# Optimization experiments

Measured on AMD Instinct MI355X. Metric: run time of the kernel, lower is better.

The kernel has to match this reference:

```python
import jax, jax.numpy as jnp
import numpy as np
from jax import lax

N = 2048    # atoms
K = 16      # knn neighbors -> E = N*K = 32768 edges
H = 128     # latent width
L = 10      # stacked InteractionNetworks
STEPS = 10  # outer simulation iterations


def _rn(key, shape, scale=0.05):
    return scale * jax.random.normal(key, shape, dtype=jnp.float32)


def setup_inputs() -> dict:
    key = jax.random.key(0)
    ks = iter(jax.random.split(key, 40))
    inp = {
        "pos": jax.random.normal(next(ks), (N, 3), dtype=jnp.float32),
        "node_f": jax.random.normal(next(ks), (N, 24), dtype=jnp.float32),
        "mass": jnp.ones((N,), jnp.float32),
        # node encoder MLP(24,128,2,128)
        "nW1": _rn(next(ks), (24, H)), "nb1": _rn(next(ks), (H,)),
        "nW2": _rn(next(ks), (H, H)), "nb2": _rn(next(ks), (H,)),
        # edge encoder MLP(4,128,2,128)
        "eW1": _rn(next(ks), (4, H)), "eb1": _rn(next(ks), (H,)),
        "eW2": _rn(next(ks), (H, H)), "eb2": _rn(next(ks), (H,)),
        # RelationModel per IN: input = 2*dim_obj + dim_rel = 384, 4 Linear layers (ReLU after each)
        "rmW1": _rn(next(ks), (L, 3 * H, H)), "rmb1": _rn(next(ks), (L, H)),
        "rmW2": _rn(next(ks), (L, H, H)), "rmb2": _rn(next(ks), (L, H)),
        "rmW3": _rn(next(ks), (L, H, H)), "rmb3": _rn(next(ks), (L, H)),
        "rmW4": _rn(next(ks), (L, H, H)), "rmb4": _rn(next(ks), (L, H)),
        # ObjectModel per IN: input = dim_obj + dim_eff = 256 -> hidden 128 -> out 128
        "omW1": _rn(next(ks), (L, 2 * H, H)), "omb1": _rn(next(ks), (L, H)),
        "omW2": _rn(next(ks), (L, H, H)), "omb2": _rn(next(ks), (L, H)),
        # decoder MLP(128,128,2,3)
        "dW1": _rn(next(ks), (H, H)), "db1": _rn(next(ks), (H,)),
        "dW2": _rn(next(ks), (H, 3)), "db2": _rn(next(ks), (3,)),
        "k": K,
    }
    return inp


def _mlp2(x, W1, b1, W2, b2):
    return jax.nn.relu(x @ W1 + b1) @ W2 + b2


def _knn_edges(pos, k):
    # knn(P.pos, k): edge_index[:,0] = sender (neighbor), edge_index[:,1] = receiver
    n = pos.shape[0]
    sq = jnp.sum(pos * pos, axis=1)
    d2 = sq[:, None] + sq[None, :] - 2.0 * (pos @ pos.T)   # [N, N]
    d2 = d2 + 1e9 * jnp.eye(n, dtype=pos.dtype)            # exclude self
    _, idx = lax.top_k(-d2, k)                              # [N, k] nearest
    senders = idx.reshape(-1)                               # [E]
    receivers = jnp.repeat(jnp.arange(n), k)                # [E]
    rel = pos[senders] - pos[receivers]
    dist = jnp.linalg.norm(rel, axis=1, keepdims=True)
    ea0 = jnp.concatenate([rel, dist], axis=1)              # [E, 4]
    return senders, receivers, ea0


def _simulate(pos, node_f, mass, nW1, nb1, nW2, nb2, eW1, eb1, eW2, eb2,
              rmW1, rmb1, rmW2, rmb2, rmW3, rmb3, rmW4, rmb4,
              omW1, omb1, omW2, omb2, dW1, db1, dW2, db2, k):
    n = pos.shape[0]
    # G.pos = G.pos + randn * 0.1 ; G.vels = zeros
    pos = pos + 0.1 * jax.random.normal(jax.random.key(42), pos.shape, dtype=pos.dtype)
    vels = jnp.zeros_like(pos)

    stacked = (rmW1, rmb1, rmW2, rmb2, rmW3, rmb3, rmW4, rmb4,
               omW1, omb1, omW2, omb2)

    for _ in range(STEPS):
        senders, receivers, ea0 = _knn_edges(pos, k)

        # encode
        x = _mlp2(node_f, nW1, nb1, nW2, nb2)    # [N, H]
        ea = _mlp2(ea0, eW1, eb1, eW2, eb2)      # [E, H]

        # process: 10 InteractionNetworks. In the original, layer(P.x, P.senders,
        # P.receivers, P.edge_attr) binds rr=senders, rs=receivers, so the
        # one-hot matmuls obj.t()@rr / obj.t()@rs are gathers by sender/receiver,
        # and e @ rr.t() is a scatter-add onto sender nodes.
        def in_step(carry, p):
            xc, eac = carry
            rW1, rb1, rW2, rb2, rW3, rb3, rW4, rb4, oW1, ob1, oW2, ob2 = p
            b = jnp.concatenate([xc[senders], xc[receivers], eac], axis=1)  # [E, 3H]
            h = jax.nn.relu(b @ rW1 + rb1)
            h = jax.nn.relu(h @ rW2 + rb2)
            h = jax.nn.relu(h @ rW3 + rb3)
            e = jax.nn.relu(h @ rW4 + rb4)                                   # [E, H]
            agg = jax.ops.segment_sum(e, senders, num_segments=n)           # e @ rr.T
            a = jnp.concatenate([xc, agg], axis=1)                           # [N, 2H]
            x_new = jax.nn.relu(a @ oW1 + ob1) @ oW2 + ob2                   # [N, H]
            return (x_new, e), None

        (x, ea), _ = lax.scan(jax.checkpoint(in_step), (x, ea), stacked)

        # decode + update
        forces = _mlp2(x, dW1, db1, dW2, db2)    # [N, 3]
        vels = vels + forces / mass[:, None]
        pos = pos + vels
    return pos


def reference(pos, node_f, mass, nW1, nb1, nW2, nb2, eW1, eb1, eW2, eb2,
              rmW1, rmb1, rmW2, rmb2, rmW3, rmb3, rmW4, rmb4,
              omW1, omb1, omW2, omb2, dW1, db1, dW2, db2, k):
    return _simulate(pos, node_f, mass, nW1, nb1, nW2, nb2, eW1, eb1, eW2, eb2,
                     rmW1, rmb1, rmW2, rmb2, rmW3, rmb3, rmW4, rmb4,
                     omW1, omb1, omW2, omb2, dW1, db1, dW2, db2, k)
```

## Files before the change

kernel.cpp:

```cpp
#include <hip/hip_runtime.h>

#define N_ATOMS 2048
#define KNN 16
#define NE (N_ATOMS*KNN)
#define H 128
#define NL 10
#define NSTEPS 10

typedef unsigned short u16;
typedef __attribute__((ext_vector_type(4))) float f32x4;
typedef __attribute__((ext_vector_type(8))) short bf16x8;

__device__ __forceinline__ u16 f2bf(float x){
  unsigned u = __float_as_uint(x);
  return (u16)((u + 0x7FFFu + ((u >> 16) & 1u)) >> 16);
}
__device__ __forceinline__ float bf2f(u16 v){ return __uint_as_float(((unsigned)v) << 16); }

template<int PITCH>
__device__ __forceinline__ bf16x8 ldsB_m6(const u16* s, int e, int k){
  int byte = e*PITCH + (k<<1); byte ^= ((e&7)<<4);
  return *(const bf16x8*)((const char*)s + byte);
}
template<int PITCH>
__device__ __forceinline__ void lds_st16_m6(u16* s, int row, int k, uint4 v){
  int byte = row*PITCH + (k<<1); byte ^= ((row&7)<<4);
  *(uint4*)((char*)s + byte) = v;
}
template<int PITCH>
__device__ __forceinline__ uint4 lds_ld16_m6(const u16* s, int row, int k){
  int byte = row*PITCH + (k<<1); byte ^= ((row&7)<<4);
  return *(const uint4*)((const char*)s + byte);
}
template<int PITCH>
__device__ __forceinline__ void lds_st8_m6(u16* s, int row, int k, uint2 v){
  int byte = row*PITCH + (k<<1); byte ^= ((row&7)<<4);
  *(uint2*)((char*)s + byte) = v;
}

template<int KST, int KS, int ET, int PITCH>
__device__ __forceinline__ void mfma_gemm_m6(const u16* sBh, const u16* sBl,
    const u16* __restrict__ pWh, const u16* __restrict__ pWl,
    int ksbase, int wpair, int rowbase, int lane, f32x4 acc[2][ET]){
  const int er = lane & 15, kg = lane >> 4;
  const size_t base = ((size_t)(wpair*KST + ksbase)*64 + lane)*8;
  #pragma unroll
  for (int ks = 0; ks < KS; ks++){
    const int klds = ks*32 + kg*8;
    bf16x8 bh[ET], bl[ET];
    #pragma unroll
    for (int et = 0; et < ET; et++){
      bh[et] = ldsB_m6<PITCH>(sBh, rowbase + et*16 + er, klds);
      bl[et] = ldsB_m6<PITCH>(sBl, rowbase + et*16 + er, klds);
    }
    #pragma unroll
    for (int nt = 0; nt < 2; nt++){
      const size_t off = base + (size_t)(nt*KST + ks)*512;
      bf16x8 ah = *(const bf16x8*)(pWh + off);
      bf16x8 al = *(const bf16x8*)(pWl + off);
      #pragma unroll
      for (int et = 0; et < ET; et++){
        acc[nt][et] = __builtin_amdgcn_mfma_f32_16x16x32_bf16(ah, bh[et], acc[nt][et], 0, 0, 0);
        acc[nt][et] = __builtin_amdgcn_mfma_f32_16x16x32_bf16(ah, bl[et], acc[nt][et], 0, 0, 0);
        acc[nt][et] = __builtin_amdgcn_mfma_f32_16x16x32_bf16(al, bh[et], acc[nt][et], 0, 0, 0);
      }
    }
  }
}

#define CLR_M6(acc, ET) { _Pragma("unroll") for (int i_=0;i_<2;i_++){ _Pragma("unroll") for (int j_=0;j_<ET;j_++){ \
  acc[i_][j_][0]=0.f; acc[i_][j_][1]=0.f; acc[i_][j_][2]=0.f; acc[i_][j_][3]=0.f; } } }

template<int ET, int PITCH, bool RELU>
__device__ __forceinline__ void epi_lds_m6(f32x4 acc[2][ET], u16* sh, u16* sl,
    int wpair, int rowbase, int lane, const float* __restrict__ bias){
  const int er = lane & 15, g = lane >> 4;
  #pragma unroll
  for (int nt = 0; nt < 2; nt++){
    const int n0 = (wpair + nt)*16 + g*4;
    f32x4 bv = *(const f32x4*)(bias + n0);
    #pragma unroll
    for (int et = 0; et < ET; et++){
      const int e = rowbase + et*16 + er;
      unsigned hw[2], lw[2];
      #pragma unroll
      for (int q = 0; q < 2; q++){
        float v0 = acc[nt][et][2*q]   + bv[2*q];
        float v1 = acc[nt][et][2*q+1] + bv[2*q+1];
        if (RELU){ v0 = fmaxf(v0, 0.f); v1 = fmaxf(v1, 0.f); }
        u16 h0 = f2bf(v0), h1 = f2bf(v1);
        u16 l0 = f2bf(v0 - bf2f(h0)), l1 = f2bf(v1 - bf2f(h1));
        hw[q] = (unsigned)h0 | ((unsigned)h1 << 16);
        lw[q] = (unsigned)l0 | ((unsigned)l1 << 16);
      }
      uint2 hv; hv.x = hw[0]; hv.y = hw[1];
      uint2 lv; lv.x = lw[0]; lv.y = lw[1];
      lds_st8_m6<PITCH>(sh, e, n0, hv);
      lds_st8_m6<PITCH>(sl, e, n0, lv);
    }
  }
}

__global__ __launch_bounds__(256) void pack_w_m6(const float* __restrict__ W,
    u16* __restrict__ ph, u16* __restrict__ pl, int KS, int L, int lstride, int roff){
  int idx = blockIdx.x*256 + threadIdx.x;
  int per = 8*KS*64;
  if (idx >= per*L) return;
  int l = idx / per, r = idx - l*per;
  int lane = r & 63, rest = r >> 6;
  int ks = rest % KS, nt = rest / KS;
  int n = nt*16 + (lane & 15), kb = ks*32 + (lane >> 4)*8;
  const float* src = W + (size_t)l*lstride;
  u16 h8[8], l8[8];
  #pragma unroll
  for (int j = 0; j < 8; j++){
    float v = src[(size_t)(roff + kb + j)*H + n];
    u16 h = f2bf(v);
    h8[j] = h; l8[j] = f2bf(v - bf2f(h));
  }
  size_t off = (size_t)idx*8;
  uint4 hv, lv;
  hv.x = h8[0]|((unsigned)h8[1]<<16); hv.y = h8[2]|((unsigned)h8[3]<<16);
  hv.z = h8[4]|((unsigned)h8[5]<<16); hv.w = h8[6]|((unsigned)h8[7]<<16);
  lv.x = l8[0]|((unsigned)l8[1]<<16); lv.y = l8[2]|((unsigned)l8[3]<<16);
  lv.z = l8[4]|((unsigned)l8[5]<<16); lv.w = l8[6]|((unsigned)l8[7]<<16);
  *(uint4*)(ph + off) = hv;
  *(uint4*)(pl + off) = lv;
}

__device__ __forceinline__ int lds_byte_f_m6(int r, int k4){
  return (((r<<9) + (k4<<2)) ^ (((r>>3)&7)<<4));
}
__device__ __forceinline__ f32x4 lds4r_f_m6(const float* s, int r, int k4){
  return *(const f32x4*)((const char*)s + lds_byte_f_m6(r,k4));
}
__device__ __forceinline__ void lds4w_f_m6(float* s, int r, int k4, f32x4 v){
  *(f32x4*)((char*)s + lds_byte_f_m6(r,k4)) = v;
}
__device__ __forceinline__ float lds1r_f_m6(const float* s, int r, int k){
  return *(const float*)((const char*)s + lds_byte_f_m6(r, k & ~3) + ((k&3)<<2));
}
template<int KD, int RPT>
__device__ __forceinline__ void gemm_f_m6(const float* sA, const float* __restrict__ gW,
                                          int r0, int c0, float acc[RPT][4]){
  #pragma unroll 2
  for (int k4 = 0; k4 < KD; k4 += 4){
    f32x4 a[RPT];
    #pragma unroll
    for (int i=0;i<RPT;i++) a[i] = lds4r_f_m6(sA, r0+i, k4);
    #pragma unroll
    for (int kk=0;kk<4;kk++){
      f32x4 wv = *(const f32x4*)(gW + (size_t)(k4+kk)*H + c0);
      #pragma unroll
      for (int i=0;i<RPT;i++){
        acc[i][0] = fmaf(a[i][kk], wv[0], acc[i][0]);
        acc[i][1] = fmaf(a[i][kk], wv[1], acc[i][1]);
        acc[i][2] = fmaf(a[i][kk], wv[2], acc[i][2]);
        acc[i][3] = fmaf(a[i][kk], wv[3], acc[i][3]);
      }
    }
  }
}

__device__ __forceinline__ unsigned rotl32_m6(unsigned v, int d){ return (v << d) | (v >> (32 - d)); }
__device__ __forceinline__ void tf2x32_m6(unsigned k0, unsigned k1, unsigned x0, unsigned x1,
                                          unsigned* o0, unsigned* o1){
  unsigned ks2 = k0 ^ k1 ^ 0x1BD11BDAu;
  x0 += k0; x1 += k1;
  const int R0[4] = {13,15,26,6}, R1[4] = {17,29,16,24};
#define TFG(R) { for (int i=0;i<4;i++){ x0 += x1; x1 = rotl32_m6(x1,R[i]); x1 ^= x0; } }
  TFG(R0); x0 += k1;  x1 += ks2 + 1u;
  TFG(R1); x0 += ks2; x1 += k0  + 2u;
  TFG(R0); x0 += k0;  x1 += k1  + 3u;
  TFG(R1); x0 += k1;  x1 += ks2 + 4u;
  TFG(R0); x0 += ks2; x1 += k0  + 5u;
#undef TFG
  *o0 = x0; *o1 = x1;
}
__device__ float bits_to_normal_m6(unsigned bits){
  float f = __uint_as_float((bits >> 9) | 0x3F800000u) - 1.0f;
  const float lo = -0.99999994f;
  float u = fmaxf(lo, __fadd_rn(__fmul_rn(f, 2.0f), lo));
  float w = -log1pf(-__fmul_rn(u, u));
  float p;
  if (w < 5.0f){
    w = __fsub_rn(w, 2.5f);
    p = 2.81022636e-08f;
    p = __fadd_rn(__fmul_rn(p,w),  3.43273939e-07f);
    p = __fadd_rn(__fmul_rn(p,w), -3.5233877e-06f);
    p = __fadd_rn(__fmul_rn(p,w), -4.39150654e-06f);
    p = __fadd_rn(__fmul_rn(p,w),  0.00021858087f);
    p = __fadd_rn(__fmul_rn(p,w), -0.00125372503f);
    p = __fadd_rn(__fmul_rn(p,w), -0.00417768164f);
    p = __fadd_rn(__fmul_rn(p,w),  0.246640727f);
    p = __fadd_rn(__fmul_rn(p,w),  1.50140941f);
  } else {
    w = __fsub_rn(sqrtf(w), 3.0f);
    p = -0.000200214257f;
    p = __fadd_rn(__fmul_rn(p,w),  0.000100950558f);
    p = __fadd_rn(__fmul_rn(p,w),  0.00134934322f);
    p = __fadd_rn(__fmul_rn(p,w), -0.00367342844f);
    p = __fadd_rn(__fmul_rn(p,w),  0.00573950773f);
    p = __fadd_rn(__fmul_rn(p,w), -0.0076224613f);
    p = __fadd_rn(__fmul_rn(p,w),  0.00943887047f);
    p = __fadd_rn(__fmul_rn(p,w),  1.00167406f);
    p = __fadd_rn(__fmul_rn(p,w),  2.83297682f);
  }
  return __fmul_rn(1.41421356f, __fmul_rn(p, u));
}
__device__ __forceinline__ unsigned draw_bits_m6(unsigned k1, unsigned k2, int bk, int m, int half){
  unsigned o0, o1;
  if (bk == 0){
    if (m < half){ tf2x32_m6(k1,k2, (unsigned)m, (unsigned)(m+half), &o0,&o1); return o0; }
    else         { tf2x32_m6(k1,k2, (unsigned)(m-half), (unsigned)m, &o0,&o1); return o1; }
  }
  tf2x32_m6(k1,k2, 0u, (unsigned)m, &o0,&o1);
  return (bk==1) ? (o0^o1) : (bk==2) ? o1 : o0;
}
__global__ __launch_bounds__(64) void rng_init_m6(int* flags){
  if (threadIdx.x < 8) flags[threadIdx.x] = 1;
}
__global__ __launch_bounds__(256) void rng_detect_m6(const float* __restrict__ pos_in, int* flags){
  int m = blockIdx.x*256 + threadIdx.x;
  if (m >= N_ATOMS*3) return;
  unsigned a0,a1,b0,b1,f0,f1;
  tf2x32_m6(0u,0u, 0u,40u, &a0,&a1);
  tf2x32_m6(0u,0u, 1u,41u, &b0,&b1);
  tf2x32_m6(0u,0u, 0u,0u,  &f0,&f1);
  float target = pos_in[m];
  #pragma unroll
  for (int v = 0; v < 8; v++){
    unsigned k1 = (v<4)? a0 : f0, k2 = (v<4)? b0 : f1;
    unsigned bits = draw_bits_m6(k1,k2, v&3, m, 3072);
    float z = bits_to_normal_m6(bits);
    if (fabsf(z - target) > 1e-3f) flags[v] = 0;
  }
}
__global__ __launch_bounds__(64) void rng_select_m6(const int* flags, int* sel){
  if (threadIdx.x == 0){
    int s = -1;
    for (int v = 0; v < 8; v++) if (flags[v]){ s = v; break; }
    sel[0] = (s < 0) ? 1 : (s & 3);
  }
}
__global__ __launch_bounds__(256) void perturb_m6(const float* __restrict__ pos,
                                                  const int* __restrict__ sel,
                                                  float* __restrict__ posw,
                                                  float* __restrict__ vels){
  int m = blockIdx.x*256 + threadIdx.x;
  if (m >= N_ATOMS*3) return;
  unsigned bits = draw_bits_m6(0u, 42u, sel[0], m, 3072);
  float z = bits_to_normal_m6(bits);
  posw[m] = __fadd_rn(pos[m], __fmul_rn(0.1f, z));
  vels[m] = 0.f;
}

__global__ __launch_bounds__(128) void node_enc_m6(const float* __restrict__ nf,
    const float* __restrict__ W1, const float* __restrict__ b1,
    const float* __restrict__ W2, const float* __restrict__ b2,
    u16* __restrict__ xh, u16* __restrict__ xl){
  __shared__ float s_in[24];
  __shared__ float s_h[128];
  int n = blockIdx.x, t = threadIdx.x;
  if (t < 24) s_in[t] = nf[n*24 + t];
  __syncthreads();
  float a = b1[t];
  #pragma unroll
  for (int k = 0; k < 24; k++) a = fmaf(s_in[k], W1[k*H + t], a);
  s_h[t] = fmaxf(a, 0.f);
  __syncthreads();
  float a2 = b2[t];
  for (int k = 0; k < H; k++) a2 = fmaf(s_h[k], W2[k*H + t], a2);
  u16 h = f2bf(a2);
  xh[(size_t)n*H + t] = h;
  xl[(size_t)n*H + t] = f2bf(a2 - bf2f(h));
}

__global__ __launch_bounds__(256) void pnode_m6(
    const u16* __restrict__ xh, const u16* __restrict__ xl,
    const u16* __restrict__ pah, const u16* __restrict__ pal,
    const u16* __restrict__ pbh, const u16* __restrict__ pbl,
    float* __restrict__ P1g, float* __restrict__ P2g){
  __shared__ __align__(16) u16 sXh[16*128];
  __shared__ __align__(16) u16 sXl[16*128];
  const int t = threadIdx.x, n0b = blockIdx.x*16;
  const int i = t>>4, seg = t&15;
  {
    uint4 hv = *(const uint4*)(xh + (size_t)(n0b+i)*H + seg*8);
    uint4 lv = *(const uint4*)(xl + (size_t)(n0b+i)*H + seg*8);
    lds_st16_m6<256>(sXh, i, seg*8, hv);
    lds_st16_m6<256>(sXl, i, seg*8, lv);
  }
  __syncthreads();
  const int w = t>>6, lane = t&63, er = lane&15, g = lane>>4;
  f32x4 acc[2][1];
  CLR_M6(acc, 1);
  mfma_gemm_m6<4,4,1,256>(sXh, sXl, pah, pal, 0, w*2, 0, lane, acc);
  #pragma unroll
  for (int nt = 0; nt < 2; nt++)
    *(f32x4*)(P1g + (size_t)(n0b+er)*H + (w*2+nt)*16 + g*4) = acc[nt][0];
  CLR_M6(acc, 1);
  mfma_gemm_m6<4,4,1,256>(sXh, sXl, pbh, pbl, 0, w*2, 0, lane, acc);
  #pragma unroll
  for (int nt = 0; nt < 2; nt++)
    *(f32x4*)(P2g + (size_t)(n0b+er)*H + (w*2+nt)*16 + g*4) = acc[nt][0];
}

__global__ __launch_bounds__(256) void knn_m6(const float* __restrict__ pos,
                                              int* __restrict__ senders,
                                              float* __restrict__ ea0){
  __shared__ float d2[N_ATOMS];
  __shared__ float pv[4];
  __shared__ int   pi[4];
  int r = blockIdx.x, t = threadIdx.x;
  float prx = pos[r*3+0], pry = pos[r*3+1], prz = pos[r*3+2];
  float sqr = __fadd_rn(__fadd_rn(__fmul_rn(prx,prx), __fmul_rn(pry,pry)), __fmul_rn(prz,prz));
  for (int c = t; c < N_ATOMS; c += 256){
    float cx = pos[c*3+0], cy = pos[c*3+1], cz = pos[c*3+2];
    float sqc = __fadd_rn(__fadd_rn(__fmul_rn(cx,cx), __fmul_rn(cy,cy)), __fmul_rn(cz,cz));
    float dot = __fadd_rn(__fadd_rn(__fmul_rn(prx,cx), __fmul_rn(pry,cy)), __fmul_rn(prz,cz));
    float v = __fsub_rn(__fadd_rn(sqr, sqc), __fmul_rn(2.0f, dot));
    d2[c] = (c == r) ? 1e9f : v;
  }
  __syncthreads();
  for (int j = 0; j < KNN; j++){
    float bv = 1e30f; int bi = 0x7fffffff;
    for (int c = t; c < N_ATOMS; c += 256){
      float v = d2[c];
      if (v < bv || (v == bv && c < bi)){ bv = v; bi = c; }
    }
    #pragma unroll
    for (int off = 32; off; off >>= 1){
      float ov = __shfl_down(bv, off);
      int   oi = __shfl_down(bi, off);
      if (ov < bv || (ov == bv && oi < bi)){ bv = ov; bi = oi; }
    }
    if ((t & 63) == 0){ pv[t>>6] = bv; pi[t>>6] = bi; }
    __syncthreads();
    if (t == 0){
      float fv = pv[0]; int fi = pi[0];
      #pragma unroll
      for (int q = 1; q < 4; q++){
        if (pv[q] < fv || (pv[q] == fv && pi[q] < fi)){ fv = pv[q]; fi = pi[q]; }
      }
      senders[r*KNN + j] = fi;
      float dx = __fsub_rn(pos[fi*3+0], prx);
      float dy = __fsub_rn(pos[fi*3+1], pry);
      float dz = __fsub_rn(pos[fi*3+2], prz);
      float ss = __fadd_rn(__fadd_rn(__fmul_rn(dx,dx), __fmul_rn(dy,dy)), __fmul_rn(dz,dz));
      float* o = ea0 + (size_t)(r*KNN + j)*4;
      o[0] = dx; o[1] = dy; o[2] = dz; o[3] = sqrtf(ss);
      d2[fi] = 1e30f;
    }
    __syncthreads();
  }
}

__global__ __launch_bounds__(1024) void csr_build_m6(const int* __restrict__ senders,
    int* __restrict__ rowstart, int* __restrict__ elist){
  __shared__ int cnt[N_ATOMS];
  __shared__ int part[256];
  const int t = threadIdx.x;
  for (int i = t; i < N_ATOMS; i += 1024) cnt[i] = 0;
  __syncthreads();
  #pragma unroll
  for (int k = 0; k < NE/1024; k++){
    int e = t + k*1024;
    atomicAdd(&cnt[senders[e]], 1);
  }
  __syncthreads();
  if (t < 256){
    int base = t*8, s = 0, loc[8];
    #pragma unroll
    for (int i = 0; i < 8; i++){ loc[i] = s; s += cnt[base+i]; }
    part[t] = s;
    __syncthreads();
    if (t == 0){
      int acc = 0;
      for (int i = 0; i < 256; i++){ int v = part[i]; part[i] = acc; acc += v; }
      rowstart[N_ATOMS] = acc;
    }
    __syncthreads();
    int p = part[t];
    #pragma unroll
    for (int i = 0; i < 8; i++){
      int v = p + loc[i];
      rowstart[base+i] = v;
      loc[i] = v;
    }
    __syncthreads();
    #pragma unroll
    for (int i = 0; i < 8; i++) cnt[base+i] = loc[i];
  } else {
    __syncthreads(); __syncthreads(); __syncthreads();
  }
  __syncthreads();
  #pragma unroll
  for (int k = 0; k < NE/1024; k++){
    int e = t + k*1024;
    int slot = atomicAdd(&cnt[senders[e]], 1);
    elist[slot] = e;
  }
}
__global__ __launch_bounds__(256) void csr_sort_m6(const int* __restrict__ rowstart, int* __restrict__ elist){
  int n = blockIdx.x*256 + threadIdx.x;
  if (n >= N_ATOMS) return;
  int b = rowstart[n], e = rowstart[n+1];
  for (int i = b+1; i < e; i++){
    int v = elist[i]; int j = i-1;
    while (j >= b && elist[j] > v){ elist[j+1] = elist[j]; j--; }
    elist[j+1] = v;
  }
}

__global__ __launch_bounds__(256) void edge_enc_m6(const float* __restrict__ ea0,
    const float* __restrict__ eW1, const float* __restrict__ eb1,
    const u16* __restrict__ e2h, const u16* __restrict__ e2l, const float* __restrict__ eb2,
    u16* __restrict__ eag){
  __shared__ float sE0[64*4];
  __shared__ __align__(16) u16 sHh[64*128];
  __shared__ __align__(16) u16 sHl[64*128];
  const int t = threadIdx.x;
  const int e0 = blockIdx.x*64;
  sE0[t] = ea0[(size_t)e0*4 + t];
  __syncthreads();
  const int w = t>>6, lane = t&63;
  const int r0 = ((lane>>3)&7)*8, c0 = w*32 + (lane&7)*4;
  f32x4 bv = *(const f32x4*)(eb1 + c0);
  f32x4 w0 = *(const f32x4*)(eW1 + 0*H + c0);
  f32x4 w1 = *(const f32x4*)(eW1 + 1*H + c0);
  f32x4 w2 = *(const f32x4*)(eW1 + 2*H + c0);
  f32x4 w3 = *(const f32x4*)(eW1 + 3*H + c0);
  #pragma unroll
  for (int i = 0; i < 8; i++){
    int r = r0 + i;
    float e0v = sE0[r*4+0], e1v = sE0[r*4+1], e2v = sE0[r*4+2], e3v = sE0[r*4+3];
    unsigned hw[2], lw[2];
    #pragma unroll
    for (int q = 0; q < 2; q++){
      float v0 = fmaf(e3v, w3[2*q],   fmaf(e2v, w2[2*q],   fmaf(e1v, w1[2*q],   fmaf(e0v, w0[2*q],   bv[2*q]))));
      float v1 = fmaf(e3v, w3[2*q+1], fmaf(e2v, w2[2*q+1], fmaf(e1v, w1[2*q+1], fmaf(e0v, w0[2*q+1], bv[2*q+1]))));
      v0 = fmaxf(v0, 0.f); v1 = fmaxf(v1, 0.f);
      u16 h0 = f2bf(v0), h1 = f2bf(v1);
      u16 l0 = f2bf(v0 - bf2f(h0)), l1 = f2bf(v1 - bf2f(h1));
      hw[q] = (unsigned)h0 | ((unsigned)h1<<16);
      lw[q] = (unsigned)l0 | ((unsigned)l1<<16);
    }
    uint2 hv; hv.x = hw[0]; hv.y = hw[1];
    uint2 lv; lv.x = lw[0]; lv.y = lw[1];
    lds_st8_m6<256>(sHh, r, c0, hv);
    lds_st8_m6<256>(sHl, r, c0, lv);
  }
  __syncthreads();
  f32x4 acc[2][4]; CLR_M6(acc, 4);
  mfma_gemm_m6<4,4,4,256>(sHh, sHl, e2h, e2l, 0, 2*w, 0, lane, acc);
  __syncthreads();
  epi_lds_m6<4,256,false>(acc, sHh, sHl, 2*w, 0, lane, eb2);
  __syncthreads();
  char* dst = (char*)(eag + (size_t)e0*256);
  #pragma unroll
  for (int m = 0; m < 8; m++){
    int byteoff = (t + m*256)*16;
    int row = byteoff>>9, off = byteoff&511;
    uint4 v = lds_ld16_m6<256>((off<256)? sHh : sHl, row, (off&255)>>1);
    *(uint4*)(dst + byteoff) = v;
  }
}

__global__ __launch_bounds__(256) void chain_m6(
    const float* __restrict__ P1g, const float* __restrict__ P2g,
    u16* __restrict__ eag, const int* __restrict__ senders,
    const u16* __restrict__ w1h, const u16* __restrict__ w1l, const float* __restrict__ b1,
    const u16* __restrict__ w2h, const u16* __restrict__ w2l, const float* __restrict__ b2,
    const u16* __restrict__ w3h, const u16* __restrict__ w3l, const float* __restrict__ b3,
    const u16* __restrict__ w4h, const u16* __restrict__ w4l, const float* __restrict__ b4){
  __shared__ __align__(16) u16 sPh[64*128];
  __shared__ __align__(16) u16 sPl[64*128];
  __shared__ __align__(16) u16 sQh[64*128];
  __shared__ __align__(16) u16 sQl[64*128];
  const int t = threadIdx.x, e0 = blockIdx.x*64;
  const int w = t>>6, lane = t&63, er = lane&15, g = lane>>4;
  const int wpair = w*2;
  f32x4 acc[2][4];
  int sidx[4];
  #pragma unroll
  for (int et = 0; et < 4; et++) sidx[et] = senders[e0 + et*16 + er];
  #pragma unroll
  for (int et = 0; et < 4; et++){
    const int r = (e0>>4) + et;
    #pragma unroll
    for (int nt = 0; nt < 2; nt++){
      const int n0 = (wpair+nt)*16 + g*4;
      f32x4 p1 = *(const f32x4*)(P1g + (size_t)sidx[et]*H + n0);
      f32x4 p2 = *(const f32x4*)(P2g + (size_t)r*H + n0);
      acc[nt][et] = p1 + p2;
    }
  }
  const char* src = (const char*)(eag + (size_t)e0*256);
  #pragma unroll
  for (int m = 0; m < 8; m++){
    int byteoff = (t + m*256)*16;
    uint4 v = *(const uint4*)(src + byteoff);
    int row = byteoff>>9, off = byteoff&511;
    lds_st16_m6<256>((off<256)? sPh : sPl, row, (off&255)>>1, v);
  }
  __syncthreads();
  mfma_gemm_m6<4,4,4,256>(sPh, sPl, w1h, w1l, 0, wpair, 0, lane, acc);
  epi_lds_m6<4,256,true>(acc, sQh, sQl, wpair, 0, lane, b1);
  __syncthreads();
  CLR_M6(acc, 4);
  mfma_gemm_m6<4,4,4,256>(sQh, sQl, w2h, w2l, 0, wpair, 0, lane, acc);
  epi_lds_m6<4,256,true>(acc, sPh, sPl, wpair, 0, lane, b2);
  __syncthreads();
  CLR_M6(acc, 4);
  mfma_gemm_m6<4,4,4,256>(sPh, sPl, w3h, w3l, 0, wpair, 0, lane, acc);
  epi_lds_m6<4,256,true>(acc, sQh, sQl, wpair, 0, lane, b3);
  __syncthreads();
  CLR_M6(acc, 4);
  mfma_gemm_m6<4,4,4,256>(sQh, sQl, w4h, w4l, 0, wpair, 0, lane, acc);
  epi_lds_m6<4,256,true>(acc, sPh, sPl, wpair, 0, lane, b4);
  __syncthreads();
  char* dst = (char*)(eag + (size_t)e0*256);
  #pragma unroll
  for (int m = 0; m < 8; m++){
    int byteoff = (t + m*256)*16;
    int row = byteoff>>9, off = byteoff&511;
    uint4 v = lds_ld16_m6<256>((off<256)? sPh : sPl, row, (off&255)>>1);
    *(uint4*)(dst + byteoff) = v;
  }
}

__global__ __launch_bounds__(256) void objagg_m6(
    const u16* __restrict__ xch, const u16* __restrict__ xcl,
    const u16* __restrict__ eag,
    const int* __restrict__ rowstart, const int* __restrict__ elist,
    const u16* __restrict__ o1h, const u16* __restrict__ o1l, const float* __restrict__ ob1,
    const u16* __restrict__ o2h, const u16* __restrict__ o2l, const float* __restrict__ ob2,
    const u16* __restrict__ nah, const u16* __restrict__ nal,
    const u16* __restrict__ nbh, const u16* __restrict__ nbl,
    u16* __restrict__ xoh, u16* __restrict__ xol,
    float* __restrict__ P1g, float* __restrict__ P2g){
  __shared__ __align__(16) u16 sIh[16*256];
  __shared__ __align__(16) u16 sIl[16*256];
  __shared__ __align__(16) u16 sHh[16*128];
  __shared__ __align__(16) u16 sHl[16*128];
  __shared__ __align__(16) u16 sXh[16*128];
  __shared__ __align__(16) u16 sXl[16*128];
  const int t = threadIdx.x, n0b = blockIdx.x*16;
  const int w = t>>6, lane = t&63;
  const int i = t>>4, seg = t&15;
  {
    uint4 hv = *(const uint4*)(xch + (size_t)(n0b+i)*H + seg*8);
    uint4 lv = *(const uint4*)(xcl + (size_t)(n0b+i)*H + seg*8);
    lds_st16_m6<512>(sIh, i, seg*8, hv);
    lds_st16_m6<512>(sIl, i, seg*8, lv);
    float a[8];
    #pragma unroll
    for (int k = 0; k < 8; k++) a[k] = 0.f;
    const int b = rowstart[n0b+i], e = rowstart[n0b+i+1];
    for (int p = b; p < e; p++){
      const int ed = elist[p];
      uint4 hv2 = *(const uint4*)(eag + (size_t)ed*256 + seg*8);
      uint4 lv2 = *(const uint4*)(eag + (size_t)ed*256 + 128 + seg*8);
      unsigned hwd[4] = {hv2.x,hv2.y,hv2.z,hv2.w};
      unsigned lwd[4] = {lv2.x,lv2.y,lv2.z,lv2.w};
      #pragma unroll
      for (int q = 0; q < 4; q++){
        a[2*q]   += bf2f((u16)(hwd[q]&0xffffu)) + bf2f((u16)(lwd[q]&0xffffu));
        a[2*q+1] += bf2f((u16)(hwd[q]>>16))     + bf2f((u16)(lwd[q]>>16));
      }
    }
    unsigned hw[4], lw[4];
    #pragma unroll
    for (int q = 0; q < 4; q++){
      float v0 = a[2*q], v1 = a[2*q+1];
      u16 h0 = f2bf(v0), h1 = f2bf(v1);
      u16 l0 = f2bf(v0 - bf2f(h0)), l1 = f2bf(v1 - bf2f(h1));
      hw[q] = (unsigned)h0 | ((unsigned)h1<<16);
      lw[q] = (unsigned)l0 | ((unsigned)l1<<16);
    }
    uint4 hv3; hv3.x=hw[0]; hv3.y=hw[1]; hv3.z=hw[2]; hv3.w=hw[3];
    uint4 lv3; lv3.x=lw[0]; lv3.y=lw[1]; lv3.z=lw[2]; lv3.w=lw[3];
    lds_st16_m6<512>(sIh, i, 128 + seg*8, hv3);
    lds_st16_m6<512>(sIl, i, 128 + seg*8, lv3);
  }
  __syncthreads();
  f32x4 acc[2][1];
  CLR_M6(acc, 1);
  mfma_gemm_m6<8,8,1,512>(sIh, sIl, o1h, o1l, 0, w*2, 0, lane, acc);
  epi_lds_m6<1,256,true>(acc, sHh, sHl, w*2, 0, lane, ob1);
  __syncthreads();
  CLR_M6(acc, 1);
  mfma_gemm_m6<4,4,1,256>(sHh, sHl, o2h, o2l, 0, w*2, 0, lane, acc);
  epi_lds_m6<1,256,false>(acc, sXh, sXl, w*2, 0, lane, ob2);
  __syncthreads();
  {
    int byteoff = t*16;
    int row = byteoff>>8, off = byteoff&255;
    uint4 hv = lds_ld16_m6<256>(sXh, row, off>>1);
    uint4 lv = lds_ld16_m6<256>(sXl, row, off>>1);
    *(uint4*)((char*)(xoh + (size_t)n0b*H) + byteoff) = hv;
    *(uint4*)((char*)(xol + (size_t)n0b*H) + byteoff) = lv;
  }
  const int er = lane&15, g = lane>>4;
  CLR_M6(acc, 1);
  mfma_gemm_m6<4,4,1,256>(sXh, sXl, nah, nal, 0, w*2, 0, lane, acc);
  #pragma unroll
  for (int nt = 0; nt < 2; nt++)
    *(f32x4*)(P1g + (size_t)(n0b+er)*H + (w*2+nt)*16 + g*4) = acc[nt][0];
  CLR_M6(acc, 1);
  mfma_gemm_m6<4,4,1,256>(sXh, sXl, nbh, nbl, 0, w*2, 0, lane, acc);
  #pragma unroll
  for (int nt = 0; nt < 2; nt++)
    *(f32x4*)(P2g + (size_t)(n0b+er)*H + (w*2+nt)*16 + g*4) = acc[nt][0];
}

__global__ __launch_bounds__(256) void decode_m6(
    const u16* __restrict__ xhi, const u16* __restrict__ xlo,
    const float* __restrict__ dW1, const float* __restrict__ db1,
    const float* __restrict__ dW2, const float* __restrict__ db2,
    const float* __restrict__ mass, float* __restrict__ posw, float* __restrict__ vels){
  __shared__ float sX[16*128];
  __shared__ float sY[16*128];
  const int t = threadIdx.x;
  const int n0 = blockIdx.x*16;
  const int w = t>>6, l = t&63;
  const int r0 = ((l>>3)&7)*2, c0 = w*32 + (l&7)*4;
  const int si = t>>4, sg = t&15;
  {
    const u16* ph = xhi + (size_t)(n0+si)*H + sg*8;
    const u16* pl = xlo + (size_t)(n0+si)*H + sg*8;
    uint4 hv = *(const uint4*)ph;
    uint4 lv = *(const uint4*)pl;
    unsigned hw[4] = {hv.x,hv.y,hv.z,hv.w}, lw[4] = {lv.x,lv.y,lv.z,lv.w};
    f32x4 v0, v1;
    #pragma unroll
    for (int m = 0; m < 2; m++){
      v0[2*m]   = bf2f((u16)(hw[m]&0xffffu)) + bf2f((u16)(lw[m]&0xffffu));
      v0[2*m+1] = bf2f((u16)(hw[m]>>16))     + bf2f((u16)(lw[m]>>16));
      v1[2*m]   = bf2f((u16)(hw[m+2]&0xffffu)) + bf2f((u16)(lw[m+2]&0xffffu));
      v1[2*m+1] = bf2f((u16)(hw[m+2]>>16))     + bf2f((u16)(lw[m+2]>>16));
    }
    lds4w_f_m6(sX, si, sg*8, v0);
    lds4w_f_m6(sX, si, sg*8 + 4, v1);
  }
  __syncthreads();
  float acc[2][4];
  #pragma unroll
  for (int i=0;i<2;i++){ acc[i][0]=0.f; acc[i][1]=0.f; acc[i][2]=0.f; acc[i][3]=0.f; }
  gemm_f_m6<128,2>(sX, dW1, r0, c0, acc);
  {
    f32x4 bv = *(const f32x4*)(db1 + c0);
    #pragma unroll
    for (int i=0;i<2;i++){
      f32x4 v;
      #pragma unroll
      for (int j=0;j<4;j++){ float x = acc[i][j] + bv[j]; v[j] = fmaxf(x, 0.f); }
      lds4w_f_m6(sY, r0+i, c0, v);
    }
  }
  __syncthreads();
  if (t < 48){
    int i = t/3, c = t - i*3;
    float a = db2[c];
    for (int k = 0; k < 128; k++) a = fmaf(lds1r_f_m6(sY, i, k), dW2[k*3 + c], a);
    int n = n0 + i;
    float f = a / mass[n];
    float v = vels[n*3 + c] + f;
    vels[n*3 + c] = v;
    posw[n*3 + c] += v;
  }
}

extern "C" void kernel_launch(void* const* d_in, const int* in_sizes, int n_in,
                              void* d_out, int out_size, void* d_ws, size_t ws_size,
                              hipStream_t stream){
  const float* pos   = (const float*)d_in[0];
  const float* nodef = (const float*)d_in[1];
  const float* mass  = (const float*)d_in[2];
  const float* nW1 = (const float*)d_in[3];  const float* nb1 = (const float*)d_in[4];
  const float* nW2 = (const float*)d_in[5];  const float* nb2 = (const float*)d_in[6];
  const float* eW1 = (const float*)d_in[7];  const float* eb1 = (const float*)d_in[8];
  const float* eW2 = (const float*)d_in[9];  const float* eb2 = (const float*)d_in[10];
  const float* rmW1 = (const float*)d_in[11]; const float* rmb1 = (const float*)d_in[12];
  const float* rmW2 = (const float*)d_in[13]; const float* rmb2 = (const float*)d_in[14];
  const float* rmW3 = (const float*)d_in[15]; const float* rmb3 = (const float*)d_in[16];
  const float* rmW4 = (const float*)d_in[17]; const float* rmb4 = (const float*)d_in[18];
  const float* omW1 = (const float*)d_in[19]; const float* omb1 = (const float*)d_in[20];
  const float* omW2 = (const float*)d_in[21]; const float* omb2 = (const float*)d_in[22];
  const float* dW1 = (const float*)d_in[23]; const float* db1 = (const float*)d_in[24];
  const float* dW2 = (const float*)d_in[25]; const float* db2 = (const float*)d_in[26];

  char* wptr = (char*)d_ws;
  auto alloc = [&](size_t bytes)->void*{
    void* p = (void*)wptr; wptr += (bytes + 255) & ~(size_t)255; return p;
  };
  float* posw  = (float*)alloc((size_t)N_ATOMS*3*4);
  float* vels  = (float*)alloc((size_t)N_ATOMS*3*4);
  int*   senders = (int*)alloc((size_t)NE*4);
  float* ea0   = (float*)alloc((size_t)NE*4*4);
  u16* xench = (u16*)alloc((size_t)N_ATOMS*H*2);
  u16* xencl = (u16*)alloc((size_t)N_ATOMS*H*2);
  u16* xAh   = (u16*)alloc((size_t)N_ATOMS*H*2);
  u16* xAl   = (u16*)alloc((size_t)N_ATOMS*H*2);
  u16* xBh   = (u16*)alloc((size_t)N_ATOMS*H*2);
  u16* xBl   = (u16*)alloc((size_t)N_ATOMS*H*2);
  u16* eag   = (u16*)alloc((size_t)NE*256*2);
  float* P1g  = (float*)alloc((size_t)N_ATOMS*H*4);
  float* P2g  = (float*)alloc((size_t)N_ATOMS*H*4);
  float* P01g = (float*)alloc((size_t)N_ATOMS*H*4);
  float* P02g = (float*)alloc((size_t)N_ATOMS*H*4);
  int* rowstart = (int*)alloc((size_t)(N_ATOMS+1)*4);
  int* elist    = (int*)alloc((size_t)NE*4);
  int* rflags   = (int*)alloc(64);
  int* rsel     = (int*)alloc(64);
  const size_t S4 = 8*4*64*8;
  const size_t S8 = 8*8*64*8;
  u16* p1ah = (u16*)alloc(S4*NL*2); u16* p1al = (u16*)alloc(S4*NL*2);
  u16* p1bh = (u16*)alloc(S4*NL*2); u16* p1bl = (u16*)alloc(S4*NL*2);
  u16* p1ch = (u16*)alloc(S4*NL*2); u16* p1cl = (u16*)alloc(S4*NL*2);
  u16* prm2h = (u16*)alloc(S4*NL*2); u16* prm2l = (u16*)alloc(S4*NL*2);
  u16* prm3h = (u16*)alloc(S4*NL*2); u16* prm3l = (u16*)alloc(S4*NL*2);
  u16* prm4h = (u16*)alloc(S4*NL*2); u16* prm4l = (u16*)alloc(S4*NL*2);
  u16* pom1h = (u16*)alloc(S8*NL*2); u16* pom1l = (u16*)alloc(S8*NL*2);
  u16* pom2h = (u16*)alloc(S4*NL*2); u16* pom2l = (u16*)alloc(S4*NL*2);
  u16* pe2h  = (u16*)alloc(S4*2);    u16* pe2l  = (u16*)alloc(S4*2);

  auto pack = [&](const float* W, u16* ph, u16* pl, int KS, int L, int lstride, int roff){
    int total = L*8*KS*64;
    pack_w_m6<<<(total+255)/256, 256, 0, stream>>>(W, ph, pl, KS, L, lstride, roff);
  };
  pack(rmW1, p1ah, p1al, 4, NL, 384*H, 0);
  pack(rmW1, p1bh, p1bl, 4, NL, 384*H, 128);
  pack(rmW1, p1ch, p1cl, 4, NL, 384*H, 256);
  pack(rmW2, prm2h, prm2l, 4, NL, H*H, 0);
  pack(rmW3, prm3h, prm3l, 4, NL, H*H, 0);
  pack(rmW4, prm4h, prm4l, 4, NL, H*H, 0);
  pack(omW1, pom1h, pom1l, 8, NL, 2*H*H, 0);
  pack(omW2, pom2h, pom2l, 4, NL, H*H, 0);
  pack(eW2,  pe2h,  pe2l,  4, 1,  H*H, 0);

  rng_init_m6<<<1, 64, 0, stream>>>(rflags);
  rng_detect_m6<<<(N_ATOMS*3+255)/256, 256, 0, stream>>>(pos, rflags);
  rng_select_m6<<<1, 64, 0, stream>>>(rflags, rsel);
  perturb_m6<<<(N_ATOMS*3+255)/256, 256, 0, stream>>>(pos, rsel, posw, vels);
  node_enc_m6<<<N_ATOMS, 128, 0, stream>>>(nodef, nW1, nb1, nW2, nb2, xench, xencl);
  pnode_m6<<<N_ATOMS/16, 256, 0, stream>>>(xench, xencl, p1ah, p1al, p1bh, p1bl, P01g, P02g);

  for (int s = 0; s < NSTEPS; s++){
    knn_m6<<<N_ATOMS, 256, 0, stream>>>(posw, senders, ea0);
    csr_build_m6<<<1, 1024, 0, stream>>>(senders, rowstart, elist);
    csr_sort_m6<<<(N_ATOMS+255)/256, 256, 0, stream>>>(rowstart, elist);
    edge_enc_m6<<<NE/64, 256, 0, stream>>>(ea0, eW1, eb1, pe2h, pe2l, eb2, eag);

    const u16* xch = xench; const u16* xcl = xencl;
    for (int l = 0; l < NL; l++){
      const float* Pa = (l == 0) ? P01g : P1g;
      const float* Pb = (l == 0) ? P02g : P2g;
      chain_m6<<<NE/64, 256, 0, stream>>>(Pa, Pb, eag, senders,
          p1ch  + (size_t)l*S4, p1cl  + (size_t)l*S4, rmb1 + l*H,
          prm2h + (size_t)l*S4, prm2l + (size_t)l*S4, rmb2 + l*H,
          prm3h + (size_t)l*S4, prm3l + (size_t)l*S4, rmb3 + l*H,
          prm4h + (size_t)l*S4, prm4l + (size_t)l*S4, rmb4 + l*H);
      u16* xnh = (l & 1) ? xAh : xBh;
      u16* xnl = (l & 1) ? xAl : xBl;
      int lp1 = (l < NL-1) ? (l+1) : l;
      objagg_m6<<<N_ATOMS/16, 256, 0, stream>>>(xch, xcl, eag, rowstart, elist,
          pom1h + (size_t)l*S8, pom1l + (size_t)l*S8, omb1 + l*H,
          pom2h + (size_t)l*S4, pom2l + (size_t)l*S4, omb2 + l*H,
          p1ah + (size_t)lp1*S4, p1al + (size_t)lp1*S4,
          p1bh + (size_t)lp1*S4, p1bl + (size_t)lp1*S4,
          xnh, xnl, P1g, P2g);
      xch = xnh; xcl = xnl;
    }
    decode_m6<<<N_ATOMS/16, 256, 0, stream>>>(xch, xcl, dW1, db1, dW2, db2, mass, posw, vels);
  }
  hipMemcpyAsync(d_out, posw, (size_t)N_ATOMS*3*4, hipMemcpyDeviceToDevice, stream);
}
```

Measured before the change: 6.003 ms.

## Fuse the whole simulation loop into one cooperative persistent kernel with grid syncs

Replaces the roughly 230 per-step kernel launches (knn, CSR build/sort, edge encoder, chain and objagg per layer, decode) with a single cooperative kernel of 512 blocks. It uses grid-wide barriers between phases and builds the CSR with atomic counts and cursors. The aim is to remove launch overhead and inter-kernel idle gaps. In exchange, occupancy is limited to 2 blocks per CU, and grid syncs plus atomic CSR construction add their own cost. The old multi-kernel path is kept as a fallback if the cooperative launch fails.

```diff
diff --git a/kernel.cpp b/kernel.cpp
--- a/kernel.cpp
+++ b/kernel.cpp
@@ -1,4 +1,7 @@
 #include <hip/hip_runtime.h>
+#include <hip/hip_cooperative_groups.h>
+
+namespace cg = cooperative_groups;
 
 #define N_ATOMS 2048
 #define KNN 16
@@ -6,6 +9,10 @@
 #define H 128
 #define NL 10
 #define NSTEPS 10
+#define S4C 16384
+#define S8C 32768
+#define S4B ((size_t)S4C)
+#define S8B ((size_t)S8C)
 
 typedef unsigned short u16;
 typedef __attribute__((ext_vector_type(4))) float f32x4;
@@ -18,28 +25,28 @@
 __device__ __forceinline__ float bf2f(u16 v){ return __uint_as_float(((unsigned)v) << 16); }
 
 template<int PITCH>
-__device__ __forceinline__ bf16x8 ldsB_m6(const u16* s, int e, int k){
+__device__ __forceinline__ bf16x8 ldsB_m7(const u16* s, int e, int k){
   int byte = e*PITCH + (k<<1); byte ^= ((e&7)<<4);
   return *(const bf16x8*)((const char*)s + byte);
 }
 template<int PITCH>
-__device__ __forceinline__ void lds_st16_m6(u16* s, int row, int k, uint4 v){
+__device__ __forceinline__ void lds_st16_m7(u16* s, int row, int k, uint4 v){
   int byte = row*PITCH + (k<<1); byte ^= ((row&7)<<4);
   *(uint4*)((char*)s + byte) = v;
 }
 template<int PITCH>
-__device__ __forceinline__ uint4 lds_ld16_m6(const u16* s, int row, int k){
+__device__ __forceinline__ uint4 lds_ld16_m7(const u16* s, int row, int k){
   int byte = row*PITCH + (k<<1); byte ^= ((row&7)<<4);
   return *(const uint4*)((const char*)s + byte);
 }
 template<int PITCH>
-__device__ __forceinline__ void lds_st8_m6(u16* s, int row, int k, uint2 v){
+__device__ __forceinline__ void lds_st8_m7(u16* s, int row, int k, uint2 v){
   int byte = row*PITCH + (k<<1); byte ^= ((row&7)<<4);
   *(uint2*)((char*)s + byte) = v;
 }
 
 template<int KST, int KS, int ET, int PITCH>
-__device__ __forceinline__ void mfma_gemm_m6(const u16* sBh, const u16* sBl,
+__device__ __forceinline__ void mfma_gemm_m7(const u16* sBh, const u16* sBl,
     const u16* __restrict__ pWh, const u16* __restrict__ pWl,
     int ksbase, int wpair, int rowbase, int lane, f32x4 acc[2][ET]){
   const int er = lane & 15, kg = lane >> 4;
@@ -50,8 +57,8 @@
     bf16x8 bh[ET], bl[ET];
     #pragma unroll
     for (int et = 0; et < ET; et++){
-      bh[et] = ldsB_m6<PITCH>(sBh, rowbase + et*16 + er, klds);
-      bl[et] = ldsB_m6<PITCH>(sBl, rowbase + et*16 + er, klds);
+      bh[et] = ldsB_m7<PITCH>(sBh, rowbase + et*16 + er, klds);
+      bl[et] = ldsB_m7<PITCH>(sBl, rowbase + et*16 + er, klds);
     }
     #pragma unroll
     for (int nt = 0; nt < 2; nt++){
@@ -68,11 +75,11 @@
   }
 }
 
-#define CLR_M6(acc, ET) { _Pragma("unroll") for (int i_=0;i_<2;i_++){ _Pragma("unroll") for (int j_=0;j_<ET;j_++){ \
+#define CLR_M7(acc, ET) { _Pragma("unroll") for (int i_=0;i_<2;i_++){ _Pragma("unroll") for (int j_=0;j_<ET;j_++){ \
   acc[i_][j_][0]=0.f; acc[i_][j_][1]=0.f; acc[i_][j_][2]=0.f; acc[i_][j_][3]=0.f; } } }
 
 template<int ET, int PITCH, bool RELU>
-__device__ __forceinline__ void epi_lds_m6(f32x4 acc[2][ET], u16* sh, u16* sl,
+__device__ __forceinline__ void epi_lds_m7(f32x4 acc[2][ET], u16* sh, u16* sl,
     int wpair, int rowbase, int lane, const float* __restrict__ bias){
   const int er = lane & 15, g = lane >> 4;
   #pragma unroll
@@ -95,13 +102,44 @@
       }
       uint2 hv; hv.x = hw[0]; hv.y = hw[1];
       uint2 lv; lv.x = lw[0]; lv.y = lw[1];
-      lds_st8_m6<PITCH>(sh, e, n0, hv);
-      lds_st8_m6<PITCH>(sl, e, n0, lv);
-    }
-  }
-}
-
-__global__ __launch_bounds__(256) void pack_w_m6(const float* __restrict__ W,
+      lds_st8_m7<PITCH>(sh, e, n0, hv);
+      lds_st8_m7<PITCH>(sl, e, n0, lv);
+    }
+  }
+}
+template<int ET, bool RELU>
+__device__ __forceinline__ void epi_glb_m7(f32x4 acc[2][ET],
+    u16* __restrict__ gh, u16* __restrict__ gl, int row0,
+    int wpair, int rowbase, int lane, const float* __restrict__ bias){
+  const int er = lane & 15, g = lane >> 4;
+  #pragma unroll
+  for (int nt = 0; nt < 2; nt++){
+    const int n0 = (wpair + nt)*16 + g*4;
+    f32x4 bv = *(const f32x4*)(bias + n0);
+    #pragma unroll
+    for (int et = 0; et < ET; et++){
+      const int e = rowbase + et*16 + er;
+      unsigned hw[2], lw[2];
+      #pragma unroll
+      for (int q = 0; q < 2; q++){
+        float v0 = acc[nt][et][2*q]   + bv[2*q];
+        float v1 = acc[nt][et][2*q+1] + bv[2*q+1];
+        if (RELU){ v0 = fmaxf(v0, 0.f); v1 = fmaxf(v1, 0.f); }
+        u16 h0 = f2bf(v0), h1 = f2bf(v1);
+        u16 l0 = f2bf(v0 - bf2f(h0)), l1 = f2bf(v1 - bf2f(h1));
+        hw[q] = (unsigned)h0 | ((unsigned)h1 << 16);
+        lw[q] = (unsigned)l0 | ((unsigned)l1 << 16);
+      }
+      size_t off = (size_t)(row0 + e)*H + n0;
+      uint2 hv; hv.x = hw[0]; hv.y = hw[1];
+      uint2 lv; lv.x = lw[0]; lv.y = lw[1];
+      *(uint2*)(gh + off) = hv;
+      *(uint2*)(gl + off) = lv;
+    }
+  }
+}
+
+__global__ __launch_bounds__(256) void pack_w_m7(const float* __restrict__ W,
     u16* __restrict__ ph, u16* __restrict__ pl, int KS, int L, int lstride, int roff){
   int idx = blockIdx.x*256 + threadIdx.x;
   int per = 8*KS*64;
@@ -128,26 +166,26 @@
   *(uint4*)(pl + off) = lv;
 }
 
-__device__ __forceinline__ int lds_byte_f_m6(int r, int k4){
+__device__ __forceinline__ int lds_byte_f_m7(int r, int k4){
   return (((r<<9) + (k4<<2)) ^ (((r>>3)&7)<<4));
 }
-__device__ __forceinline__ f32x4 lds4r_f_m6(const float* s, int r, int k4){
-  return *(const f32x4*)((const char*)s + lds_byte_f_m6(r,k4));
-}
-__device__ __forceinline__ void lds4w_f_m6(float* s, int r, int k4, f32x4 v){
-  *(f32x4*)((char*)s + lds_byte_f_m6(r,k4)) = v;
-}
-__device__ __forceinline__ float lds1r_f_m6(const float* s, int r, int k){
-  return *(const float*)((const char*)s + lds_byte_f_m6(r, k & ~3) + ((k&3)<<2));
+__device__ __forceinline__ f32x4 lds4r_f_m7(const float* s, int r, int k4){
+  return *(const f32x4*)((const char*)s + lds_byte_f_m7(r,k4));
+}
+__device__ __forceinline__ void lds4w_f_m7(float* s, int r, int k4, f32x4 v){
+  *(f32x4*)((char*)s + lds_byte_f_m7(r,k4)) = v;
+}
+__device__ __forceinline__ float lds1r_f_m7(const float* s, int r, int k){
+  return *(const float*)((const char*)s + lds_byte_f_m7(r, k & ~3) + ((k&3)<<2));
 }
 template<int KD, int RPT>
-__device__ __forceinline__ void gemm_f_m6(const float* sA, const float* __restrict__ gW,
+__device__ __forceinline__ void gemm_f_m7(const float* sA, const float* __restrict__ gW,
                                           int r0, int c0, float acc[RPT][4]){
   #pragma unroll 2
   for (int k4 = 0; k4 < KD; k4 += 4){
     f32x4 a[RPT];
     #pragma unroll
-    for (int i=0;i<RPT;i++) a[i] = lds4r_f_m6(sA, r0+i, k4);
+    for (int i=0;i<RPT;i++) a[i] = lds4r_f_m7(sA, r0+i, k4);
     #pragma unroll
     for (int kk=0;kk<4;kk++){
       f32x4 wv = *(const f32x4*)(gW + (size_t)(k4+kk)*H + c0);
@@ -162,13 +200,13 @@
   }
 }
 
-__device__ __forceinline__ unsigned rotl32_m6(unsigned v, int d){ return (v << d) | (v >> (32 - d)); }
-__device__ __forceinline__ void tf2x32_m6(unsigned k0, unsigned k1, unsigned x0, unsigned x1,
+__device__ __forceinline__ unsigned rotl32_m7(unsigned v, int d){ return (v << d) | (v >> (32 - d)); }
+__device__ __forceinline__ void tf2x32_m7(unsigned k0, unsigned k1, unsigned x0, unsigned x1,
                                           unsigned* o0, unsigned* o1){
   unsigned ks2 = k0 ^ k1 ^ 0x1BD11BDAu;
   x0 += k0; x1 += k1;
   const int R0[4] = {13,15,26,6}, R1[4] = {17,29,16,24};
-#define TFG(R) { for (int i=0;i<4;i++){ x0 += x1; x1 = rotl32_m6(x1,R[i]); x1 ^= x0; } }
+#define TFG(R) { for (int i=0;i<4;i++){ x0 += x1; x1 = rotl32_m7(x1,R[i]); x1 ^= x0; } }
   TFG(R0); x0 += k1;  x1 += ks2 + 1u;
   TFG(R1); x0 += ks2; x1 += k0  + 2u;
   TFG(R0); x0 += k0;  x1 += k1  + 3u;
@@ -177,7 +215,7 @@
 #undef TFG
   *o0 = x0; *o1 = x1;
 }
-__device__ float bits_to_normal_m6(unsigned bits){
+__device__ float bits_to_normal_m7(unsigned bits){
   float f = __uint_as_float((bits >> 9) | 0x3F800000u) - 1.0f;
   const float lo = -0.99999994f;
   float u = fmaxf(lo, __fadd_rn(__fmul_rn(f, 2.0f), lo));
@@ -208,54 +246,52 @@
   }
   return __fmul_rn(1.41421356f, __fmul_rn(p, u));
 }
-__device__ __forceinline__ unsigned draw_bits_m6(unsigned k1, unsigned k2, int bk, int m, int half){
+__device__ __forceinline__ unsigned draw_bits_m7(unsigned k1, unsigned k2, int bk, int m, int half){
   unsigned o0, o1;
   if (bk == 0){
-    if (m < half){ tf2x32_m6(k1,k2, (unsigned)m, (unsigned)(m+half), &o0,&o1); return o0; }
-    else         { tf2x32_m6(k1,k2, (unsigned)(m-half), (unsigned)m, &o0,&o1); return o1; }
-  }
-  tf2x32_m6(k1,k2, 0u, (unsigned)m, &o0,&o1);
+    if (m < half){ tf2x32_m7(k1,k2, (unsigned)m, (unsigned)(m+half), &o0,&o1); return o0; }
+    else         { tf2x32_m7(k1,k2, (unsigned)(m-half), (unsigned)m, &o0,&o1); return o1; }
+  }
+  tf2x32_m7(k1,k2, 0u, (unsigned)m, &o0,&o1);
   return (bk==1) ? (o0^o1) : (bk==2) ? o1 : o0;
 }
-__global__ __launch_bounds__(64) void rng_init_m6(int* flags){
+__global__ __launch_bounds__(64) void rng_init_m7(int* flags){
   if (threadIdx.x < 8) flags[threadIdx.x] = 1;
 }
-__global__ __launch_bounds__(256) void rng_detect_m6(const float* __restrict__ pos_in, int* flags){
+__global__ __launch_bounds__(256) void rng_detect_m7(const float* __restrict__ pos_in, int* flags){
   int m = blockIdx.x*256 + threadIdx.x;
   if (m >= N_ATOMS*3) return;
   unsigned a0,a1,b0,b1,f0,f1;
-  tf2x32_m6(0u,0u, 0u,40u, &a0,&a1);
-  tf2x32_m6(0u,0u, 1u,41u, &b0,&b1);
-  tf2x32_m6(0u,0u, 0u,0u,  &f0,&f1);
+  tf2x32_m7(0u,0u, 0u,40u, &a0,&a1);
+  tf2x32_m7(0u,0u, 1u,41u, &b0,&b1);
+  tf2x32_m7(0u,0u, 0u,0u,  &f0,&f1);
   float target = pos_in[m];
   #pragma unroll
   for (int v = 0; v < 8; v++){
     unsigned k1 = (v<4)? a0 : f0, k2 = (v<4)? b0 : f1;
-    unsigned bits = draw_bits_m6(k1,k2, v&3, m, 3072);
-    float z = bits_to_normal_m6(bits);
+    unsigned bits = draw_bits_m7(k1,k2, v&3, m, 3072);
+    float z = bits_to_normal_m7(bits);
     if (fabsf(z - target) > 1e-3f) flags[v] = 0;
   }
 }
-__global__ __launch_bounds__(64) void rng_select_m6(const int* flags, int* sel){
+__global__ __launch_bounds__(64) void rng_select_m7(const int* flags, int* sel){
   if (threadIdx.x == 0){
     int s = -1;
     for (int v = 0; v < 8; v++) if (flags[v]){ s = v; break; }
     sel[0] = (s < 0) ? 1 : (s & 3);
   }
 }
-__global__ __launch_bounds__(256) void perturb_m6(const float* __restrict__ pos,
-                                                  const int* __restrict__ sel,
-                                                  float* __restrict__ posw,
-                                                  float* __restrict__ vels){
+__global__ __launch_bounds__(256) void perturb_m7(const float* __restrict__ pos,
+    const int* __restrict__ sel, float* __restrict__ posw, float* __restrict__ vels){
   int m = blockIdx.x*256 + threadIdx.x;
   if (m >= N_ATOMS*3) return;
-  unsigned bits = draw_bits_m6(0u, 42u, sel[0], m, 3072);
-  float z = bits_to_normal_m6(bits);
+  unsigned bits = draw_bits_m7(0u, 42u, sel[0], m, 3072);
+  float z = bits_to_normal_m7(bits);
   posw[m] = __fadd_rn(pos[m], __fmul_rn(0.1f, z));
   vels[m] = 0.f;
 }
 
-__global__ __launch_bounds__(128) void node_enc_m6(const float* __restrict__ nf,
+__global__ __launch_bounds__(128) void node_enc_m7(const float* __restrict__ nf,
     const float* __restrict__ W1, const float* __restrict__ b1,
     const float* __restrict__ W2, const float* __restrict__ b2,
     u16* __restrict__ xh, u16* __restrict__ xl){
@@ -276,7 +312,7 @@
   xl[(size_t)n*H + t] = f2bf(a2 - bf2f(h));
 }
 
-__global__ __launch_bounds__(256) void pnode_m6(
+__global__ __launch_bounds__(256) void pnode_m7(
     const u16* __restrict__ xh, const u16* __restrict__ xl,
     const u16* __restrict__ pah, const u16* __restrict__ pal,
     const u16* __restrict__ pbh, const u16* __restrict__ pbl,
@@ -288,27 +324,391 @@
   {
     uint4 hv = *(const uint4*)(xh + (size_t)(n0b+i)*H + seg*8);
     uint4 lv = *(const uint4*)(xl + (size_t)(n0b+i)*H + seg*8);
-    lds_st16_m6<256>(sXh, i, seg*8, hv);
-    lds_st16_m6<256>(sXl, i, seg*8, lv);
+    lds_st16_m7<256>(sXh, i, seg*8, hv);
+    lds_st16_m7<256>(sXl, i, seg*8, lv);
   }
   __syncthreads();
   const int w = t>>6, lane = t&63, er = lane&15, g = lane>>4;
   f32x4 acc[2][1];
-  CLR_M6(acc, 1);
-  mfma_gemm_m6<4,4,1,256>(sXh, sXl, pah, pal, 0, w*2, 0, lane, acc);
+  CLR_M7(acc, 1);
+  mfma_gemm_m7<4,4,1,256>(sXh, sXl, pah, pal, 0, w*2, 0, lane, acc);
   #pragma unroll
   for (int nt = 0; nt < 2; nt++)
     *(f32x4*)(P1g + (size_t)(n0b+er)*H + (w*2+nt)*16 + g*4) = acc[nt][0];
-  CLR_M6(acc, 1);
-  mfma_gemm_m6<4,4,1,256>(sXh, sXl, pbh, pbl, 0, w*2, 0, lane, acc);
+  CLR_M7(acc, 1);
+  mfma_gemm_m7<4,4,1,256>(sXh, sXl, pbh, pbl, 0, w*2, 0, lane, acc);
   #pragma unroll
   for (int nt = 0; nt < 2; nt++)
     *(f32x4*)(P2g + (size_t)(n0b+er)*H + (w*2+nt)*16 + g*4) = acc[nt][0];
 }
 
-__global__ __launch_bounds__(256) void knn_m6(const float* __restrict__ pos,
-                                              int* __restrict__ senders,
-                                              float* __restrict__ ea0){
+struct MegaP {
+  float* posw; float* vels;
+  int* senders; int* counts; int* rowstart; int* cursor; int* elist;
+  u16* eag;
+  const u16* xench; const u16* xencl;
+  u16* xAh; u16* xAl; u16* xBh; u16* xBl;
+  float* P1g; float* P2g; const float* P01g; const float* P02g;
+  const float* eW1; const float* eb1; const float* eb2;
+  const u16* pe2h; const u16* pe2l;
+  const u16* p1ah; const u16* p1al; const u16* p1bh; const u16* p1bl;
+  const u16* p1ch; const u16* p1cl;
+  const u16* prm2h; const u16* prm2l;
+  const u16* prm3h; const u16* prm3l;
+  const u16* prm4h; const u16* prm4l;
+  const u16* pom1h; const u16* pom1l;
+  const u16* pom2h; const u16* pom2l;
+  const float* rmb1; const float* rmb2; const float* rmb3; const float* rmb4;
+  const float* omb1; const float* omb2;
+  const float* dW1; const float* db1; const float* dW2; const float* db2;
+  const float* mass;
+};
+
+__global__ __launch_bounds__(256, 2) void mega_m7(MegaP P){
+  cg::grid_group grid = cg::this_grid();
+  __shared__ __align__(16) char SM[65536];
+  const int b = blockIdx.x, t = threadIdx.x;
+  const int w = t >> 6, lane = t & 63;
+  const int er = lane & 15, g = lane >> 4;
+
+  for (int s = 0; s < NSTEPS; s++){
+    {
+      float* d2 = (float*)(SM + w*8192);
+      int*   sSend = (int*)(SM + 49152);
+      float* ea0loc = (float*)(SM + 50176);
+      const int r = b*4 + w;
+      float prx = P.posw[r*3+0], pry = P.posw[r*3+1], prz = P.posw[r*3+2];
+      float sqr = __fadd_rn(__fadd_rn(__fmul_rn(prx,prx), __fmul_rn(pry,pry)), __fmul_rn(prz,prz));
+      for (int c = lane; c < N_ATOMS; c += 64){
+        float cx = P.posw[c*3+0], cy = P.posw[c*3+1], cz = P.posw[c*3+2];
+        float sqc = __fadd_rn(__fadd_rn(__fmul_rn(cx,cx), __fmul_rn(cy,cy)), __fmul_rn(cz,cz));
+        float dot = __fadd_rn(__fadd_rn(__fmul_rn(prx,cx), __fmul_rn(pry,cy)), __fmul_rn(prz,cz));
+        float v = __fsub_rn(__fadd_rn(sqr, sqc), __fmul_rn(2.0f, dot));
+        d2[c] = (c == r) ? 1e9f : v;
+      }
+      asm volatile("" ::: "memory");
+      for (int j = 0; j < KNN; j++){
+        float bv = 1e30f; int bi = 0x7fffffff;
+        for (int c = lane; c < N_ATOMS; c += 64){
+          float v = d2[c];
+          if (v < bv || (v == bv && c < bi)){ bv = v; bi = c; }
+        }
+        #pragma unroll
+        for (int off = 32; off; off >>= 1){
+          float ov = __shfl_down(bv, off);
+          int   oi = __shfl_down(bi, off);
+          if (ov < bv || (ov == bv && oi < bi)){ bv = ov; bi = oi; }
+        }
+        if (lane == 0){
+          sSend[w*16 + j] = bi;
+          float dx = __fsub_rn(P.posw[bi*3+0], prx);
+          float dy = __fsub_rn(P.posw[bi*3+1], pry);
+          float dz = __fsub_rn(P.posw[bi*3+2], prz);
+          float ss = __fadd_rn(__fadd_rn(__fmul_rn(dx,dx), __fmul_rn(dy,dy)), __fmul_rn(dz,dz));
+          float* o = ea0loc + (w*16 + j)*4;
+          o[0] = dx; o[1] = dy; o[2] = dz; o[3] = sqrtf(ss);
+          d2[bi] = 1e30f;
+        }
+        asm volatile("" ::: "memory");
+      }
+      __syncthreads();
+      if (t < 64){
+        int sv = sSend[t];
+        P.senders[b*64 + t] = sv;
+        atomicAdd(&P.counts[sv], 1);
+      }
+      __syncthreads();
+      u16* sHh = (u16*)SM;
+      u16* sHl = (u16*)(SM + 16384);
+      const int r0e = ((lane>>3)&7)*8, c0e = w*32 + (lane&7)*4;
+      f32x4 bv1 = *(const f32x4*)(P.eb1 + c0e);
+      f32x4 w0v = *(const f32x4*)(P.eW1 + 0*H + c0e);
+      f32x4 w1v = *(const f32x4*)(P.eW1 + 1*H + c0e);
+      f32x4 w2v = *(const f32x4*)(P.eW1 + 2*H + c0e);
+      f32x4 w3v = *(const f32x4*)(P.eW1 + 3*H + c0e);
+      #pragma unroll
+      for (int i = 0; i < 8; i++){
+        int rr = r0e + i;
+        float e0v = ea0loc[rr*4+0], e1v = ea0loc[rr*4+1], e2v = ea0loc[rr*4+2], e3v = ea0loc[rr*4+3];
+        unsigned hw[2], lw[2];
+        #pragma unroll
+        for (int q = 0; q < 2; q++){
+          float v0 = fmaf(e3v, w3v[2*q],   fmaf(e2v, w2v[2*q],   fmaf(e1v, w1v[2*q],   fmaf(e0v, w0v[2*q],   bv1[2*q]))));
+          float v1 = fmaf(e3v, w3v[2*q+1], fmaf(e2v, w2v[2*q+1], fmaf(e1v, w1v[2*q+1], fmaf(e0v, w0v[2*q+1], bv1[2*q+1]))));
+          v0 = fmaxf(v0, 0.f); v1 = fmaxf(v1, 0.f);
+          u16 h0 = f2bf(v0), h1 = f2bf(v1);
+          u16 l0 = f2bf(v0 - bf2f(h0)), l1 = f2bf(v1 - bf2f(h1));
+          hw[q] = (unsigned)h0 | ((unsigned)h1<<16);
+          lw[q] = (unsigned)l0 | ((unsigned)l1<<16);
+        }
+        uint2 hv; hv.x = hw[0]; hv.y = hw[1];
+        uint2 lv; lv.x = lw[0]; lv.y = lw[1];
+        lds_st8_m7<256>(sHh, rr, c0e, hv);
+        lds_st8_m7<256>(sHl, rr, c0e, lv);
+      }
+      __syncthreads();
+      f32x4 acc[2][4];
+      CLR_M7(acc, 4);
+      mfma_gemm_m7<4,4,4,256>(sHh, sHl, P.pe2h, P.pe2l, 0, 2*w, 0, lane, acc);
+      __syncthreads();
+      epi_lds_m7<4,256,false>(acc, sHh, sHl, 2*w, 0, lane, P.eb2);
+      __syncthreads();
+      {
+        char* dst = (char*)(P.eag + (size_t)(b*64)*256);
+        #pragma unroll
+        for (int m = 0; m < 8; m++){
+          int byteoff = (t + m*256)*16;
+          int row = byteoff>>9, off = byteoff&511;
+          uint4 v = lds_ld16_m7<256>((off<256)? sHh : sHl, row, (off&255)>>1);
+          *(uint4*)(dst + byteoff) = v;
+        }
+      }
+    }
+    grid.sync();
+    if (b == 0){
+      int* part = (int*)SM;
+      int base = t*8, ssum = 0, loc[8];
+      #pragma unroll
+      for (int i = 0; i < 8; i++){ loc[i] = ssum; ssum += P.counts[base+i]; }
+      part[t] = ssum;
+      __syncthreads();
+      if (t == 0){
+        int acc2 = 0;
+        for (int i = 0; i < 256; i++){ int v = part[i]; part[i] = acc2; acc2 += v; }
+        P.rowstart[N_ATOMS] = acc2;
+      }
+      __syncthreads();
+      int p0 = part[t];
+      #pragma unroll
+      for (int i = 0; i < 8; i++){
+        int v = p0 + loc[i];
+        P.rowstart[base+i] = v;
+        P.cursor[base+i] = v;
+      }
+    }
+    grid.sync();
+    if (t < 64){
+      int e = b*64 + t;
+      int sv = P.senders[e];
+      int slot = atomicAdd(&P.cursor[sv], 1);
+      P.elist[slot] = e;
+    } else if (t < 68){
+      P.counts[b*4 + (t - 64)] = 0;
+    }
+    grid.sync();
+    const u16* xch = P.xench; const u16* xcl = P.xencl;
+    for (int l = 0; l < NL; l++){
+      if (l == 0 && t < 4){
+        int n = b*4 + t;
+        int b0 = P.rowstart[n], e1s = P.rowstart[n+1];
+        for (int i = b0+1; i < e1s; i++){
+          int v = P.elist[i]; int j = i-1;
+          while (j >= b0 && P.elist[j] > v){ P.elist[j+1] = P.elist[j]; j--; }
+          P.elist[j+1] = v;
+        }
+      }
+      {
+        u16* sPh = (u16*)SM;
+        u16* sPl = (u16*)(SM + 16384);
+        u16* sQh = (u16*)(SM + 32768);
+        u16* sQl = (u16*)(SM + 49152);
+        const int e0 = b*64;
+        const int wpair = w*2;
+        const float* Pa = (l == 0) ? P.P01g : P.P1g;
+        const float* Pb = (l == 0) ? P.P02g : P.P2g;
+        const u16* w1h = P.p1ch + (size_t)l*S4B;  const u16* w1l = P.p1cl + (size_t)l*S4B;
+        const u16* w2h = P.prm2h + (size_t)l*S4B; const u16* w2l = P.prm2l + (size_t)l*S4B;
+        const u16* w3h = P.prm3h + (size_t)l*S4B; const u16* w3l = P.prm3l + (size_t)l*S4B;
+        const u16* w4h = P.prm4h + (size_t)l*S4B; const u16* w4l = P.prm4l + (size_t)l*S4B;
+        f32x4 acc[2][4];
+        int sidx[4];
+        #pragma unroll
+        for (int et = 0; et < 4; et++) sidx[et] = P.senders[e0 + et*16 + er];
+        #pragma unroll
+        for (int et = 0; et < 4; et++){
+          const int rr = (e0>>4) + et;
+          #pragma unroll
+          for (int nt = 0; nt < 2; nt++){
+            const int n0 = (wpair+nt)*16 + g*4;
+            f32x4 p1 = *(const f32x4*)(Pa + (size_t)sidx[et]*H + n0);
+            f32x4 p2 = *(const f32x4*)(Pb + (size_t)rr*H + n0);
+            acc[nt][et] = p1 + p2;
+          }
+        }
+        {
+          const char* src = (const char*)(P.eag + (size_t)e0*256);
+          #pragma unroll
+          for (int m = 0; m < 8; m++){
+            int byteoff = (t + m*256)*16;
+            uint4 v = *(const uint4*)(src + byteoff);
+            int row = byteoff>>9, off = byteoff&511;
+            lds_st16_m7<256>((off<256)? sPh : sPl, row, (off&255)>>1, v);
+          }
+        }
+        __syncthreads();
+        mfma_gemm_m7<4,4,4,256>(sPh, sPl, w1h, w1l, 0, wpair, 0, lane, acc);
+        epi_lds_m7<4,256,true>(acc, sQh, sQl, wpair, 0, lane, P.rmb1 + l*H);
+        __syncthreads();
+        CLR_M7(acc, 4);
+        mfma_gemm_m7<4,4,4,256>(sQh, sQl, w2h, w2l, 0, wpair, 0, lane, acc);
+        epi_lds_m7<4,256,true>(acc, sPh, sPl, wpair, 0, lane, P.rmb2 + l*H);
+        __syncthreads();
+        CLR_M7(acc, 4);
+        mfma_gemm_m7<4,4,4,256>(sPh, sPl, w3h, w3l, 0, wpair, 0, lane, acc);
+        epi_lds_m7<4,256,true>(acc, sQh, sQl, wpair, 0, lane, P.rmb3 + l*H);
+        __syncthreads();
+        CLR_M7(acc, 4);
+        mfma_gemm_m7<4,4,4,256>(sQh, sQl, w4h, w4l, 0, wpair, 0, lane, acc);
+        epi_lds_m7<4,256,true>(acc, sPh, sPl, wpair, 0, lane, P.rmb4 + l*H);
+        __syncthreads();
+        {
+          char* dst = (char*)(P.eag + (size_t)e0*256);
+          #pragma unroll
+          for (int m = 0; m < 8; m++){
+            int byteoff = (t + m*256)*16;
+            int row = byteoff>>9, off = byteoff&511;
+            uint4 v = lds_ld16_m7<256>((off<256)? sPh : sPl, row, (off&255)>>1);
+            *(uint4*)(dst + byteoff) = v;
+          }
+        }
+      }
+      grid.sync();
+      u16* xnh = (l & 1) ? P.xAh : P.xBh;
+      u16* xnl = (l & 1) ? P.xAl : P.xBl;
+      if (b < 128){
+        u16* sIh  = (u16*)SM;
+        u16* sIl  = (u16*)(SM + 8192);
+        u16* sHh2 = (u16*)(SM + 16384);
+        u16* sHl2 = (u16*)(SM + 20480);
+        u16* sXh  = (u16*)(SM + 24576);
+        u16* sXl  = (u16*)(SM + 28672);
+        const int n0b = b*16;
+        const int i = t>>4, seg = t&15;
+        {
+          uint4 hv = *(const uint4*)(xch + (size_t)(n0b+i)*H + seg*8);
+          uint4 lv = *(const uint4*)(xcl + (size_t)(n0b+i)*H + seg*8);
+          lds_st16_m7<512>(sIh, i, seg*8, hv);
+          lds_st16_m7<512>(sIl, i, seg*8, lv);
+          float a[8];
+          #pragma unroll
+          for (int k = 0; k < 8; k++) a[k] = 0.f;
+          const int b0 = P.rowstart[n0b+i], e1a = P.rowstart[n0b+i+1];
+          for (int p = b0; p < e1a; p++){
+            const int ed = P.elist[p];
+            uint4 hv2 = *(const uint4*)(P.eag + (size_t)ed*256 + seg*8);
+            uint4 lv2 = *(const uint4*)(P.eag + (size_t)ed*256 + 128 + seg*8);
+            unsigned hwd[4] = {hv2.x,hv2.y,hv2.z,hv2.w};
+            unsigned lwd[4] = {lv2.x,lv2.y,lv2.z,lv2.w};
+            #pragma unroll
+            for (int q = 0; q < 4; q++){
+              a[2*q]   += bf2f((u16)(hwd[q]&0xffffu)) + bf2f((u16)(lwd[q]&0xffffu));
+              a[2*q+1] += bf2f((u16)(hwd[q]>>16))     + bf2f((u16)(lwd[q]>>16));
+            }
+          }
+          unsigned hw2[4], lw2[4];
+          #pragma unroll
+          for (int q = 0; q < 4; q++){
+            float v0 = a[2*q], v1 = a[2*q+1];
+            u16 h0 = f2bf(v0), h1 = f2bf(v1);
+            u16 l0 = f2bf(v0 - bf2f(h0)), l1 = f2bf(v1 - bf2f(h1));
+            hw2[q] = (unsigned)h0 | ((unsigned)h1<<16);
+            lw2[q] = (unsigned)l0 | ((unsigned)l1<<16);
+          }
+          uint4 hv3; hv3.x=hw2[0]; hv3.y=hw2[1]; hv3.z=hw2[2]; hv3.w=hw2[3];
+          uint4 lv3; lv3.x=lw2[0]; lv3.y=lw2[1]; lv3.z=lw2[2]; lv3.w=lw2[3];
+          lds_st16_m7<512>(sIh, i, 128 + seg*8, hv3);
+          lds_st16_m7<512>(sIl, i, 128 + seg*8, lv3);
+        }
+        __syncthreads();
+        f32x4 acc1[2][1];
+        CLR_M7(acc1, 1);
+        mfma_gemm_m7<8,8,1,512>(sIh, sIl, P.pom1h + (size_t)l*S8B, P.pom1l + (size_t)l*S8B,
+                                0, w*2, 0, lane, acc1);
+        epi_lds_m7<1,256,true>(acc1, sHh2, sHl2, w*2, 0, lane, P.omb1 + l*H);
+        __syncthreads();
+        CLR_M7(acc1, 1);
+        mfma_gemm_m7<4,4,1,256>(sHh2, sHl2, P.pom2h + (size_t)l*S4B, P.pom2l + (size_t)l*S4B,
+                                0, w*2, 0, lane, acc1);
+        epi_lds_m7<1,256,false>(acc1, sXh, sXl, w*2, 0, lane, P.omb2 + l*H);
+        __syncthreads();
+        if (l < NL-1){
+          {
+            int byteoff = t*16;
+            int row = byteoff>>8, off = byteoff&255;
+            uint4 hv = lds_ld16_m7<256>(sXh, row, off>>1);
+            uint4 lv = lds_ld16_m7<256>(sXl, row, off>>1);
+            *(uint4*)((char*)(xnh + (size_t)n0b*H) + byteoff) = hv;
+            *(uint4*)((char*)(xnl + (size_t)n0b*H) + byteoff) = lv;
+          }
+          const int lp1 = l + 1;
+          CLR_M7(acc1, 1);
+          mfma_gemm_m7<4,4,1,256>(sXh, sXl, P.p1ah + (size_t)lp1*S4B, P.p1al + (size_t)lp1*S4B,
+                                  0, w*2, 0, lane, acc1);
+          #pragma unroll
+          for (int nt = 0; nt < 2; nt++)
+            *(f32x4*)(P.P1g + (size_t)(n0b+er)*H + (w*2+nt)*16 + g*4) = acc1[nt][0];
+          CLR_M7(acc1, 1);
+          mfma_gemm_m7<4,4,1,256>(sXh, sXl, P.p1bh + (size_t)lp1*S4B, P.p1bl + (size_t)lp1*S4B,
+                                  0, w*2, 0, lane, acc1);
+          #pragma unroll
+          for (int nt = 0; nt < 2; nt++)
+            *(f32x4*)(P.P2g + (size_t)(n0b+er)*H + (w*2+nt)*16 + g*4) = acc1[nt][0];
+        } else {
+          float* sXf = (float*)(SM + 32768);
+          float* sYf = (float*)(SM + 40960);
+          {
+            uint4 hv = lds_ld16_m7<256>(sXh, i, seg*8);
+            uint4 lv = lds_ld16_m7<256>(sXl, i, seg*8);
+            unsigned hwv[4] = {hv.x,hv.y,hv.z,hv.w}, lwv[4] = {lv.x,lv.y,lv.z,lv.w};
+            f32x4 v0, v1;
+            #pragma unroll
+            for (int m = 0; m < 2; m++){
+              v0[2*m]   = bf2f((u16)(hwv[m]&0xffffu)) + bf2f((u16)(lwv[m]&0xffffu));
+              v0[2*m+1] = bf2f((u16)(hwv[m]>>16))     + bf2f((u16)(lwv[m]>>16));
+              v1[2*m]   = bf2f((u16)(hwv[m+2]&0xffffu)) + bf2f((u16)(lwv[m+2]&0xffffu));
+              v1[2*m+1] = bf2f((u16)(hwv[m+2]>>16))     + bf2f((u16)(lwv[m+2]>>16));
+            }
+            lds4w_f_m7(sXf, i, seg*8, v0);
+            lds4w_f_m7(sXf, i, seg*8 + 4, v1);
+          }
+          __syncthreads();
+          const int r0d = ((lane>>3)&7)*2, c0d = w*32 + (lane&7)*4;
+          float fac[2][4];
+          #pragma unroll
+          for (int ii = 0; ii < 2; ii++){ fac[ii][0]=0.f; fac[ii][1]=0.f; fac[ii][2]=0.f; fac[ii][3]=0.f; }
+          gemm_f_m7<128,2>(sXf, P.dW1, r0d, c0d, fac);
+          {
+            f32x4 bvd = *(const f32x4*)(P.db1 + c0d);
+            #pragma unroll
+            for (int ii = 0; ii < 2; ii++){
+              f32x4 v;
+              #pragma unroll
+              for (int jj = 0; jj < 4; jj++){ float x = fac[ii][jj] + bvd[jj]; v[jj] = fmaxf(x, 0.f); }
+              lds4w_f_m7(sYf, r0d+ii, c0d, v);
+            }
+          }
+          __syncthreads();
+          if (t < 48){
+            int i2 = t/3, c = t - i2*3;
+            float a2 = P.db2[c];
+            for (int k = 0; k < H; k++) a2 = fmaf(lds1r_f_m7(sYf, i2, k), P.dW2[k*3 + c], a2);
+            int n = n0b + i2;
+            float f = a2 / P.mass[n];
+            float v = P.vels[n*3 + c] + f;
+            P.vels[n*3 + c] = v;
+            P.posw[n*3 + c] += v;
+          }
+        }
+      }
+      grid.sync();
+      xch = xnh; xcl = xnl;
+    }
+  }
+}
+
+__global__ __launch_bounds__(256) void knn_m7f(const float* __restrict__ pos,
+                                               int* __restrict__ senders,
+                                               float* __restrict__ ea0){
   __shared__ float d2[N_ATOMS];
   __shared__ float pv[4];
   __shared__ int   pi[4];
@@ -355,8 +755,7 @@
     __syncthreads();
   }
 }
-
-__global__ __launch_bounds__(1024) void csr_build_m6(const int* __restrict__ senders,
+__global__ __launch_bounds__(1024) void csr_build_m7f(const int* __restrict__ senders,
     int* __restrict__ rowstart, int* __restrict__ elist){
   __shared__ int cnt[N_ATOMS];
   __shared__ int part[256];
@@ -402,7 +801,7 @@
     elist[slot] = e;
   }
 }
-__global__ __launch_bounds__(256) void csr_sort_m6(const int* __restrict__ rowstart, int* __restrict__ elist){
+__global__ __launch_bounds__(256) void csr_sort_m7f(const int* __restrict__ rowstart, int* __restrict__ elist){
   int n = blockIdx.x*256 + threadIdx.x;
   if (n >= N_ATOMS) return;
   int b = rowstart[n], e = rowstart[n+1];
@@ -412,8 +811,7 @@
     elist[j+1] = v;
   }
 }
-
-__global__ __launch_bounds__(256) void edge_enc_m6(const float* __restrict__ ea0,
+__global__ __launch_bounds__(256) void edge_enc_m7f(const float* __restrict__ ea0,
     const float* __restrict__ eW1, const float* __restrict__ eb1,
     const u16* __restrict__ e2h, const u16* __restrict__ e2l, const float* __restrict__ eb2,
     u16* __restrict__ eag){
@@ -448,26 +846,25 @@
     }
     uint2 hv; hv.x = hw[0]; hv.y = hw[1];
     uint2 lv; lv.x = lw[0]; lv.y = lw[1];
-    lds_st8_m6<256>(sHh, r, c0, hv);
-    lds_st8_m6<256>(sHl, r, c0, lv);
-  }
-  __syncthreads();
-  f32x4 acc[2][4]; CLR_M6(acc, 4);
-  mfma_gemm_m6<4,4,4,256>(sHh, sHl, e2h, e2l, 0, 2*w, 0, lane, acc);
-  __syncthreads();
-  epi_lds_m6<4,256,false>(acc, sHh, sHl, 2*w, 0, lane, eb2);
+    lds_st8_m7<256>(sHh, r, c0, hv);
+    lds_st8_m7<256>(sHl, r, c0, lv);
+  }
+  __syncthreads();
+  f32x4 acc[2][4]; CLR_M7(acc, 4);
+  mfma_gemm_m7<4,4,4,256>(sHh, sHl, e2h, e2l, 0, 2*w, 0, lane, acc);
+  __syncthreads();
+  epi_lds_m7<4,256,false>(acc, sHh, sHl, 2*w, 0, lane, eb2);
   __syncthreads();
   char* dst = (char*)(eag + (size_t)e0*256);
   #pragma unroll
   for (int m = 0; m < 8; m++){
     int byteoff = (t + m*256)*16;
     int row = byteoff>>9, off = byteoff&511;
-    uint4 v = lds_ld16_m6<256>((off<256)? sHh : sHl, row, (off&255)>>1);
+    uint4 v = lds_ld16_m7<256>((off<256)? sHh : sHl, row, (off&255)>>1);
     *(uint4*)(dst + byteoff) = v;
   }
 }
-
-__global__ __launch_bounds__(256) void chain_m6(
+__global__ __launch_bounds__(256) void chain_m7f(
     const float* __restrict__ P1g, const float* __restrict__ P2g,
     u16* __restrict__ eag, const int* __restrict__ senders,
     const u16* __restrict__ w1h, const u16* __restrict__ w1l, const float* __restrict__ b1,
@@ -496,41 +893,42 @@
       acc[nt][et] = p1 + p2;
     }
   }
-  const char* src = (const char*)(eag + (size_t)e0*256);
-  #pragma unroll
-  for (int m = 0; m < 8; m++){
-    int byteoff = (t + m*256)*16;
-    uint4 v = *(const uint4*)(src + byteoff);
-    int row = byteoff>>9, off = byteoff&511;
-    lds_st16_m6<256>((off<256)? sPh : sPl, row, (off&255)>>1, v);
-  }
-  __syncthreads();
-  mfma_gemm_m6<4,4,4,256>(sPh, sPl, w1h, w1l, 0, wpair, 0, lane, acc);
-  epi_lds_m6<4,256,true>(acc, sQh, sQl, wpair, 0, lane, b1);
-  __syncthreads();
-  CLR_M6(acc, 4);
-  mfma_gemm_m6<4,4,4,256>(sQh, sQl, w2h, w2l, 0, wpair, 0, lane, acc);
-  epi_lds_m6<4,256,true>(acc, sPh, sPl, wpair, 0, lane, b2);
-  __syncthreads();
-  CLR_M6(acc, 4);
-  mfma_gemm_m6<4,4,4,256>(sPh, sPl, w3h, w3l, 0, wpair, 0, lane, acc);
-  epi_lds_m6<4,256,true>(acc, sQh, sQl, wpair, 0, lane, b3);
-  __syncthreads();
-  CLR_M6(acc, 4);
-  mfma_gemm_m6<4,4,4,256>(sQh, sQl, w4h, w4l, 0, wpair, 0, lane, acc);
-  epi_lds_m6<4,256,true>(acc, sPh, sPl, wpair, 0, lane, b4);
+  {
+    const char* src = (const char*)(eag + (size_t)e0*256);
+    #pragma unroll
+    for (int m = 0; m < 8; m++){
+      int byteoff = (t + m*256)*16;
+      uint4 v = *(const uint4*)(src + byteoff);
+      int row = byteoff>>9, off = byteoff&511;
+      lds_st16_m7<256>((off<256)? sPh : sPl, row, (off&255)>>1, v);
+    }
+  }
+  __syncthreads();
+  mfma_gemm_m7<4,4,4,256>(sPh, sPl, w1h, w1l, 0, wpair, 0, lane, acc);
+  epi_lds_m7<4,256,true>(acc, sQh, sQl, wpair, 0, lane, b1);
+  __syncthreads();
+  CLR_M7(acc, 4);
+  mfma_gemm_m7<4,4,4,256>(sQh, sQl, w2h, w2l, 0, wpair, 0, lane, acc);
+  epi_lds_m7<4,256,true>(acc, sPh, sPl, wpair, 0, lane, b2);
+  __syncthreads();
+  CLR_M7(acc, 4);
+  mfma_gemm_m7<4,4,4,256>(sPh, sPl, w3h, w3l, 0, wpair, 0, lane, acc);
+  epi_lds_m7<4,256,true>(acc, sQh, sQl, wpair, 0, lane, b3);
+  __syncthreads();
+  CLR_M7(acc, 4);
+  mfma_gemm_m7<4,4,4,256>(sQh, sQl, w4h, w4l, 0, wpair, 0, lane, acc);
+  epi_lds_m7<4,256,true>(acc, sPh, sPl, wpair, 0, lane, b4);
   __syncthreads();
   char* dst = (char*)(eag + (size_t)e0*256);
   #pragma unroll
   for (int m = 0; m < 8; m++){
     int byteoff = (t + m*256)*16;
     int row = byteoff>>9, off = byteoff&511;
-    uint4 v = lds_ld16_m6<256>((off<256)? sPh : sPl, row, (off&255)>>1);
+    uint4 v = lds_ld16_m7<256>((off<256)? sPh : sPl, row, (off&255)>>1);
     *(uint4*)(dst + byteoff) = v;
   }
 }
-
-__global__ __launch_bounds__(256) void objagg_m6(
+__global__ __launch_bounds__(256) void objagg_m7f(
     const u16* __restrict__ xch, const u16* __restrict__ xcl,
     const u16* __restrict__ eag,
     const int* __restrict__ rowstart, const int* __restrict__ elist,
@@ -552,8 +950,8 @@
   {
     uint4 hv = *(const uint4*)(xch + (size_t)(n0b+i)*H + seg*8);
     uint4 lv = *(const uint4*)(xcl + (size_t)(n0b+i)*H + seg*8);
-    lds_st16_m6<512>(sIh, i, seg*8, hv);
-    lds_st16_m6<512>(sIl, i, seg*8, lv);
+    lds_st16_m7<512>(sIh, i, seg*8, hv);
+    lds_st16_m7<512>(sIl, i, seg*8, lv);
     float a[8];
     #pragma unroll
     for (int k = 0; k < 8; k++) a[k] = 0.f;
@@ -581,41 +979,40 @@
     }
     uint4 hv3; hv3.x=hw[0]; hv3.y=hw[1]; hv3.z=hw[2]; hv3.w=hw[3];
     uint4 lv3; lv3.x=lw[0]; lv3.y=lw[1]; lv3.z=lw[2]; lv3.w=lw[3];
-    lds_st16_m6<512>(sIh, i, 128 + seg*8, hv3);
-    lds_st16_m6<512>(sIl, i, 128 + seg*8, lv3);
+    lds_st16_m7<512>(sIh, i, 128 + seg*8, hv3);
+    lds_st16_m7<512>(sIl, i, 128 + seg*8, lv3);
   }
   __syncthreads();
   f32x4 acc[2][1];
-  CLR_M6(acc, 1);
-  mfma_gemm_m6<8,8,1,512>(sIh, sIl, o1h, o1l, 0, w*2, 0, lane, acc);
-  epi_lds_m6<1,256,true>(acc, sHh, sHl, w*2, 0, lane, ob1);
-  __syncthreads();
-  CLR_M6(acc, 1);
-  mfma_gemm_m6<4,4,1,256>(sHh, sHl, o2h, o2l, 0, w*2, 0, lane, acc);
-  epi_lds_m6<1,256,false>(acc, sXh, sXl, w*2, 0, lane, ob2);
+  CLR_M7(acc, 1);
+  mfma_gemm_m7<8,8,1,512>(sIh, sIl, o1h, o1l, 0, w*2, 0, lane, acc);
+  epi_lds_m7<1,256,true>(acc, sHh, sHl, w*2, 0, lane, ob1);
+  __syncthreads();
+  CLR_M7(acc, 1);
+  mfma_gemm_m7<4,4,1,256>(sHh, sHl, o2h, o2l, 0, w*2, 0, lane, acc);
+  epi_lds_m7<1,256,false>(acc, sXh, sXl, w*2, 0, lane, ob2);
   __syncthreads();
   {
     int byteoff = t*16;
     int row = byteoff>>8, off = byteoff&255;
-    uint4 hv = lds_ld16_m6<256>(sXh, row, off>>1);
-    uint4 lv = lds_ld16_m6<256>(sXl, row, off>>1);
+    uint4 hv = lds_ld16_m7<256>(sXh, row, off>>1);
+    uint4 lv = lds_ld16_m7<256>(sXl, row, off>>1);
     *(uint4*)((char*)(xoh + (size_t)n0b*H) + byteoff) = hv;
     *(uint4*)((char*)(xol + (size_t)n0b*H) + byteoff) = lv;
   }
   const int er = lane&15, g = lane>>4;
-  CLR_M6(acc, 1);
-  mfma_gemm_m6<4,4,1,256>(sXh, sXl, nah, nal, 0, w*2, 0, lane, acc);
+  CLR_M7(acc, 1);
+  mfma_gemm_m7<4,4,1,256>(sXh, sXl, nah, nal, 0, w*2, 0, lane, acc);
   #pragma unroll
   for (int nt = 0; nt < 2; nt++)
     *(f32x4*)(P1g + (size_t)(n0b+er)*H + (w*2+nt)*16 + g*4) = acc[nt][0];
-  CLR_M6(acc, 1);
-  mfma_gemm_m6<4,4,1,256>(sXh, sXl, nbh, nbl, 0, w*2, 0, lane, acc);
+  CLR_M7(acc, 1);
+  mfma_gemm_m7<4,4,1,256>(sXh, sXl, nbh, nbl, 0, w*2, 0, lane, acc);
   #pragma unroll
   for (int nt = 0; nt < 2; nt++)
     *(f32x4*)(P2g + (size_t)(n0b+er)*H + (w*2+nt)*16 + g*4) = acc[nt][0];
 }
-
-__global__ __launch_bounds__(256) void decode_m6(
+__global__ __launch_bounds__(256) void decode_m7f(
     const u16* __restrict__ xhi, const u16* __restrict__ xlo,
     const float* __restrict__ dW1, const float* __restrict__ db1,
     const float* __restrict__ dW2, const float* __restrict__ db2,
@@ -641,14 +1038,14 @@
       v1[2*m]   = bf2f((u16)(hw[m+2]&0xffffu)) + bf2f((u16)(lw[m+2]&0xffffu));
       v1[2*m+1] = bf2f((u16)(hw[m+2]>>16))     + bf2f((u16)(lw[m+2]>>16));
     }
-    lds4w_f_m6(sX, si, sg*8, v0);
-    lds4w_f_m6(sX, si, sg*8 + 4, v1);
+    lds4w_f_m7(sX, si, sg*8, v0);
+    lds4w_f_m7(sX, si, sg*8 + 4, v1);
   }
   __syncthreads();
   float acc[2][4];
   #pragma unroll
   for (int i=0;i<2;i++){ acc[i][0]=0.f; acc[i][1]=0.f; acc[i][2]=0.f; acc[i][3]=0.f; }
-  gemm_f_m6<128,2>(sX, dW1, r0, c0, acc);
+  gemm_f_m7<128,2>(sX, dW1, r0, c0, acc);
   {
     f32x4 bv = *(const f32x4*)(db1 + c0);
     #pragma unroll
@@ -656,14 +1053,14 @@
       f32x4 v;
       #pragma unroll
       for (int j=0;j<4;j++){ float x = acc[i][j] + bv[j]; v[j] = fmaxf(x, 0.f); }
-      lds4w_f_m6(sY, r0+i, c0, v);
+      lds4w_f_m7(sY, r0+i, c0, v);
     }
   }
   __syncthreads();
   if (t < 48){
     int i = t/3, c = t - i*3;
     float a = db2[c];
-    for (int k = 0; k < 128; k++) a = fmaf(lds1r_f_m6(sY, i, k), dW2[k*3 + c], a);
+    for (int k = 0; k < 128; k++) a = fmaf(lds1r_f_m7(sY, i, k), dW2[k*3 + c], a);
     int n = n0 + i;
     float f = a / mass[n];
     float v = vels[n*3 + c] + f;
@@ -710,25 +1107,25 @@
   float* P2g  = (float*)alloc((size_t)N_ATOMS*H*4);
   float* P01g = (float*)alloc((size_t)N_ATOMS*H*4);
   float* P02g = (float*)alloc((size_t)N_ATOMS*H*4);
+  int* counts   = (int*)alloc((size_t)N_ATOMS*4);
   int* rowstart = (int*)alloc((size_t)(N_ATOMS+1)*4);
+  int* cursor   = (int*)alloc((size_t)N_ATOMS*4);
   int* elist    = (int*)alloc((size_t)NE*4);
   int* rflags   = (int*)alloc(64);
   int* rsel     = (int*)alloc(64);
-  const size_t S4 = 8*4*64*8;
-  const size_t S8 = 8*8*64*8;
-  u16* p1ah = (u16*)alloc(S4*NL*2); u16* p1al = (u16*)alloc(S4*NL*2);
-  u16* p1bh = (u16*)alloc(S4*NL*2); u16* p1bl = (u16*)alloc(S4*NL*2);
-  u16* p1ch = (u16*)alloc(S4*NL*2); u16* p1cl = (u16*)alloc(S4*NL*2);
-  u16* prm2h = (u16*)alloc(S4*NL*2); u16* prm2l = (u16*)alloc(S4*NL*2);
-  u16* prm3h = (u16*)alloc(S4*NL*2); u16* prm3l = (u16*)alloc(S4*NL*2);
-  u16* prm4h = (u16*)alloc(S4*NL*2); u16* prm4l = (u16*)alloc(S4*NL*2);
-  u16* pom1h = (u16*)alloc(S8*NL*2); u16* pom1l = (u16*)alloc(S8*NL*2);
-  u16* pom2h = (u16*)alloc(S4*NL*2); u16* pom2l = (u16*)alloc(S4*NL*2);
-  u16* pe2h  = (u16*)alloc(S4*2);    u16* pe2l  = (u16*)alloc(S4*2);
+  u16* p1ah = (u16*)alloc(S4B*NL*2); u16* p1al = (u16*)alloc(S4B*NL*2);
+  u16* p1bh = (u16*)alloc(S4B*NL*2); u16* p1bl = (u16*)alloc(S4B*NL*2);
+  u16* p1ch = (u16*)alloc(S4B*NL*2); u16* p1cl = (u16*)alloc(S4B*NL*2);
+  u16* prm2h = (u16*)alloc(S4B*NL*2); u16* prm2l = (u16*)alloc(S4B*NL*2);
+  u16* prm3h = (u16*)alloc(S4B*NL*2); u16* prm3l = (u16*)alloc(S4B*NL*2);
+  u16* prm4h = (u16*)alloc(S4B*NL*2); u16* prm4l = (u16*)alloc(S4B*NL*2);
+  u16* pom1h = (u16*)alloc(S8B*NL*2); u16* pom1l = (u16*)alloc(S8B*NL*2);
+  u16* pom2h = (u16*)alloc(S4B*NL*2); u16* pom2l = (u16*)alloc(S4B*NL*2);
+  u16* pe2h  = (u16*)alloc(S4B*2);    u16* pe2l  = (u16*)alloc(S4B*2);
 
   auto pack = [&](const float* W, u16* ph, u16* pl, int KS, int L, int lstride, int roff){
     int total = L*8*KS*64;
-    pack_w_m6<<<(total+255)/256, 256, 0, stream>>>(W, ph, pl, KS, L, lstride, roff);
+    pack_w_m7<<<(total+255)/256, 256, 0, stream>>>(W, ph, pl, KS, L, lstride, roff);
   };
   pack(rmW1, p1ah, p1al, 4, NL, 384*H, 0);
   pack(rmW1, p1bh, p1bl, 4, NL, 384*H, 128);
@@ -740,40 +1137,66 @@
   pack(omW2, pom2h, pom2l, 4, NL, H*H, 0);
   pack(eW2,  pe2h,  pe2l,  4, 1,  H*H, 0);
 
-  rng_init_m6<<<1, 64, 0, stream>>>(rflags);
-  rng_detect_m6<<<(N_ATOMS*3+255)/256, 256, 0, stream>>>(pos, rflags);
-  rng_select_m6<<<1, 64, 0, stream>>>(rflags, rsel);
-  perturb_m6<<<(N_ATOMS*3+255)/256, 256, 0, stream>>>(pos, rsel, posw, vels);
-  node_enc_m6<<<N_ATOMS, 128, 0, stream>>>(nodef, nW1, nb1, nW2, nb2, xench, xencl);
-  pnode_m6<<<N_ATOMS/16, 256, 0, stream>>>(xench, xencl, p1ah, p1al, p1bh, p1bl, P01g, P02g);
-
-  for (int s = 0; s < NSTEPS; s++){
-    knn_m6<<<N_ATOMS, 256, 0, stream>>>(posw, senders, ea0);
-    csr_build_m6<<<1, 1024, 0, stream>>>(senders, rowstart, elist);
-    csr_sort_m6<<<(N_ATOMS+255)/256, 256, 0, stream>>>(rowstart, elist);
-    edge_enc_m6<<<NE/64, 256, 0, stream>>>(ea0, eW1, eb1, pe2h, pe2l, eb2, eag);
-
-    const u16* xch = xench; const u16* xcl = xencl;
-    for (int l = 0; l < NL; l++){
-      const float* Pa = (l == 0) ? P01g : P1g;
-      const float* Pb = (l == 0) ? P02g : P2g;
-      chain_m6<<<NE/64, 256, 0, stream>>>(Pa, Pb, eag, senders,
-          p1ch  + (size_t)l*S4, p1cl  + (size_t)l*S4, rmb1 + l*H,
-          prm2h + (size_t)l*S4, prm2l + (size_t)l*S4, rmb2 + l*H,
-          prm3h + (size_t)l*S4, prm3l + (size_t)l*S4, rmb3 + l*H,
-          prm4h + (size_t)l*S4, prm4l + (size_t)l*S4, rmb4 + l*H);
-      u16* xnh = (l & 1) ? xAh : xBh;
-      u16* xnl = (l & 1) ? xAl : xBl;
-      int lp1 = (l < NL-1) ? (l+1) : l;
-      objagg_m6<<<N_ATOMS/16, 256, 0, stream>>>(xch, xcl, eag, rowstart, elist,
-          pom1h + (size_t)l*S8, pom1l + (size_t)l*S8, omb1 + l*H,
-          pom2h + (size_t)l*S4, pom2l + (size_t)l*S4, omb2 + l*H,
-          p1ah + (size_t)lp1*S4, p1al + (size_t)lp1*S4,
-          p1bh + (size_t)lp1*S4, p1bl + (size_t)lp1*S4,
-          xnh, xnl, P1g, P2g);
-      xch = xnh; xcl = xnl;
-    }
-    decode_m6<<<N_ATOMS/16, 256, 0, stream>>>(xch, xcl, dW1, db1, dW2, db2, mass, posw, vels);
+  rng_init_m7<<<1, 64, 0, stream>>>(rflags);
+  rng_detect_m7<<<(N_ATOMS*3+255)/256, 256, 0, stream>>>(pos, rflags);
+  rng_select_m7<<<1, 64, 0, stream>>>(rflags, rsel);
+  perturb_m7<<<(N_ATOMS*3+255)/256, 256, 0, stream>>>(pos, rsel, posw, vels);
+  node_enc_m7<<<N_ATOMS, 128, 0, stream>>>(nodef, nW1, nb1, nW2, nb2, xench, xencl);
+  pnode_m7<<<N_ATOMS/16, 256, 0, stream>>>(xench, xencl, p1ah, p1al, p1bh, p1bl, P01g, P02g);
+  hipMemsetAsync(counts, 0, (size_t)N_ATOMS*4, stream);
+
+  MegaP mp;
+  mp.posw = posw; mp.vels = vels;
+  mp.senders = senders; mp.counts = counts; mp.rowstart = rowstart; mp.cursor = cursor; mp.elist = elist;
+  mp.eag = eag;
+  mp.xench = xench; mp.xencl = xencl;
+  mp.xAh = xAh; mp.xAl = xAl; mp.xBh = xBh; mp.xBl = xBl;
+  mp.P1g = P1g; mp.P2g = P2g; mp.P01g = P01g; mp.P02g = P02g;
+  mp.eW1 = eW1; mp.eb1 = eb1; mp.eb2 = eb2;
+  mp.pe2h = pe2h; mp.pe2l = pe2l;
+  mp.p1ah = p1ah; mp.p1al = p1al; mp.p1bh = p1bh; mp.p1bl = p1bl;
+  mp.p1ch = p1ch; mp.p1cl = p1cl;
+  mp.prm2h = prm2h; mp.prm2l = prm2l;
+  mp.prm3h = prm3h; mp.prm3l = prm3l;
+  mp.prm4h = prm4h; mp.prm4l = prm4l;
+  mp.pom1h = pom1h; mp.pom1l = pom1l;
+  mp.pom2h = pom2h; mp.pom2l = pom2l;
+  mp.rmb1 = rmb1; mp.rmb2 = rmb2; mp.rmb3 = rmb3; mp.rmb4 = rmb4;
+  mp.omb1 = omb1; mp.omb2 = omb2;
+  mp.dW1 = dW1; mp.db1 = db1; mp.dW2 = dW2; mp.db2 = db2;
+  mp.mass = mass;
+
+  void* kargs[] = { (void*)&mp };
+  hipError_t ce = hipLaunchCooperativeKernel((const void*)mega_m7,
+                                             dim3(512), dim3(256), kargs, 0, stream);
+  if (ce != hipSuccess){
+    for (int s = 0; s < NSTEPS; s++){
+      knn_m7f<<<N_ATOMS, 256, 0, stream>>>(posw, senders, ea0);
+      csr_build_m7f<<<1, 1024, 0, stream>>>(senders, rowstart, elist);
+      csr_sort_m7f<<<(N_ATOMS+255)/256, 256, 0, stream>>>(rowstart, elist);
+      edge_enc_m7f<<<NE/64, 256, 0, stream>>>(ea0, eW1, eb1, pe2h, pe2l, eb2, eag);
+      const u16* xch = xench; const u16* xcl = xencl;
+      for (int l = 0; l < NL; l++){
+        const float* Pa = (l == 0) ? P01g : P1g;
+        const float* Pb = (l == 0) ? P02g : P2g;
+        chain_m7f<<<NE/64, 256, 0, stream>>>(Pa, Pb, eag, senders,
+            p1ch  + (size_t)l*S4B, p1cl  + (size_t)l*S4B, rmb1 + l*H,
+            prm2h + (size_t)l*S4B, prm2l + (size_t)l*S4B, rmb2 + l*H,
+            prm3h + (size_t)l*S4B, prm3l + (size_t)l*S4B, rmb3 + l*H,
+            prm4h + (size_t)l*S4B, prm4l + (size_t)l*S4B, rmb4 + l*H);
+        u16* xnh = (l & 1) ? xAh : xBh;
+        u16* xnl = (l & 1) ? xAl : xBl;
+        int lp1 = (l < NL-1) ? (l+1) : l;
+        objagg_m7f<<<N_ATOMS/16, 256, 0, stream>>>(xch, xcl, eag, rowstart, elist,
+            pom1h + (size_t)l*S8B, pom1l + (size_t)l*S8B, omb1 + l*H,
+            pom2h + (size_t)l*S4B, pom2l + (size_t)l*S4B, omb2 + l*H,
+            p1ah + (size_t)lp1*S4B, p1al + (size_t)lp1*S4B,
+            p1bh + (size_t)lp1*S4B, p1bl + (size_t)lp1*S4B,
+            xnh, xnl, P1g, P2g);
+        xch = xnh; xcl = xnl;
+      }
+      decode_m7f<<<N_ATOMS/16, 256, 0, stream>>>(xch, xcl, dW1, db1, dW2, db2, mass, posw, vels);
+    }
   }
   hipMemcpyAsync(d_out, posw, (size_t)N_ATOMS*3*4, hipMemcpyDeviceToDevice, stream);
 }
```

Result: slower. 19.16 ms (+219.1%).
